# Kernel optimization log

Hardware: AMD Instinct MI355X
Metric: run time of the kernel (lower is better)

Reference implementation:

```python
import jax, jax.numpy as jnp
import numpy as np
import math

P = 2; GS = 64; TPS = 32; T = TPS * TPS; DIM = 256; NH = 8; HD = DIM // NH; NL = 5; FFH = 1024
SCALES = ((0.15, 16), (0.3, 32))
ENC_H = 32; ENC_O = 64
XMIN, XMAX, YMIN, YMAX = -2.0, 4.0, -1.5, 1.5
NFREQ = 10
N_PTS = 20000; N_Q = 100000; G = GS * GS


def rope_tables():
    half = HD // 2
    inv = 1.0 / (10000.0 ** (jnp.arange(0, half, 2, dtype=jnp.float32) / half))  # [HD/4]
    h = jnp.arange(TPS, dtype=jnp.float32)
    w = jnp.arange(TPS, dtype=jnp.float32)
    hg, wg = jnp.meshgrid(h, w, indexing='ij')
    ax = wg.reshape(-1)[:, None] * inv[None, :]  # [T, HD/4]
    ay = hg.reshape(-1)[:, None] * inv[None, :]
    return jnp.cos(ax), jnp.sin(ax), jnp.cos(ay), jnp.sin(ay)


def apply_rope(x, cx, sx, cy, sy):
    B, H, Tn, D = x.shape
    hd = D // 2; pd = hd // 2
    xp = x[..., :hd].reshape(B, H, Tn, pd, 2)
    yp = x[..., hd:].reshape(B, H, Tn, pd, 2)
    cx = cx[None, None]; sx = sx[None, None]; cy = cy[None, None]; sy = sy[None, None]
    rx = jnp.stack([xp[..., 0] * cx - xp[..., 1] * sx, xp[..., 0] * sx + xp[..., 1] * cx], -1).reshape(B, H, Tn, hd)
    ry = jnp.stack([yp[..., 0] * cy - yp[..., 1] * sy, yp[..., 0] * sy + yp[..., 1] * cy], -1).reshape(B, H, Tn, hd)
    return jnp.concatenate([rx, ry], -1)


def rmsnorm(x, w):
    n = jax.lax.rsqrt(jnp.mean(x.astype(jnp.float32) ** 2, -1, keepdims=True) + 1e-6)
    return (x.astype(jnp.float32) * n).astype(x.dtype) * w


def encode_scale(grid, points, radius, k, w1, b1, w2, b2):
    # squared distances [G, N] via gemm (monotone in euclidean dist -> same topk)
    g2 = jnp.sum(grid ** 2, -1, keepdims=True)
    p2 = jnp.sum(points ** 2, -1)
    d2 = g2 + p2[None, :] - 2.0 * (grid @ points.T)
    neg, idx = jax.lax.top_k(-d2, k)  # k nearest
    valid = (-neg) < radius * radius  # [G, k]
    rel = points[idx] - grid[:, None, :]  # [G, k, 2]
    rel = jnp.where(valid[..., None], rel, 0.0)
    h = jax.nn.relu(rel @ w1 + b1)
    f = h @ w2 + b2  # [G, k, ENC_O]
    masked = jnp.where(valid[..., None], f, -jnp.inf)
    pooled = jnp.max(masked, axis=1)
    return jnp.where(jnp.any(valid, axis=1)[:, None], pooled, 0.0)


def fourier_feats(x):
    freqs = (2.0 ** jnp.arange(NFREQ, dtype=jnp.float32)) * math.pi
    scaled = x[..., None] * freqs  # [..., 2, NFREQ]
    enc = jnp.concatenate([jnp.sin(scaled), jnp.cos(scaled)], -1).reshape(*x.shape[:-1], -1)
    return jnp.concatenate([x, enc], -1)  # [..., 2*(1+2*NFREQ)]


def bilinear_sample(feat, xn, yn):
    # feat [C,H,W]; xn,yn in [-1,1]; align_corners=True, border padding
    C, H, W = feat.shape
    px = (xn + 1.0) * 0.5 * (W - 1)
    py = (yn + 1.0) * 0.5 * (H - 1)
    x0 = jnp.clip(jnp.floor(px), 0, W - 1)
    y0 = jnp.clip(jnp.floor(py), 0, H - 1)
    wx = px - x0; wy = py - y0
    x0i = x0.astype(jnp.int32); y0i = y0.astype(jnp.int32)
    x1i = jnp.clip(x0i + 1, 0, W - 1); y1i = jnp.clip(y0i + 1, 0, H - 1)
    f00 = feat[:, y0i, x0i]; f01 = feat[:, y0i, x1i]
    f10 = feat[:, y1i, x0i]; f11 = feat[:, y1i, x1i]
    out = (f00 * (1 - wx) * (1 - wy) + f01 * wx * (1 - wy) + f10 * (1 - wx) * wy + f11 * wx * wy)
    return out.T  # [N, C]


def forward(points, grid, query_pos, query_uinf, query_sdf, query_sdf_grad,
            enc_w1, enc_b1, enc_w2, enc_b2, inproj_w, inproj_b, patch_w, patch_b,
            norm1_w, qkv_w, attnproj_w, norm2_w, gate_w, value_w, ffnout_w,
            unpatch_w, unpatch_b, posmlp_w1, posmlp_b1, posmlp_w2, posmlp_b2,
            pred_w1, pred_b1, pred_w2, pred_b2):
    # --- PointNet multi-scale encoder onto grid ---
    feats = [encode_scale(grid, points, SCALES[i][0], SCALES[i][1],
                          enc_w1[i], enc_b1[i], enc_w2[i], enc_b2[i]) for i in range(len(SCALES))]
    gfeat = jnp.concatenate(feats, -1) @ inproj_w + inproj_b  # [G, DIM]
    img = gfeat.reshape(GS, GS, DIM).transpose(2, 0, 1)[None]  # [1, DIM, GS, GS]
    # --- patchify ---
    x = img.reshape(1, DIM, TPS, P, TPS, P).transpose(0, 2, 4, 1, 3, 5).reshape(1, T, DIM * P * P)
    tok = x @ patch_w + patch_b  # [1, T, DIM]
    cx, sx, cy, sy = rope_tables()
    scale = 1.0 / math.sqrt(HD)
    for l in range(NL):
        h = rmsnorm(tok, norm1_w[l])
        qkv = (h @ qkv_w[l]).reshape(1, T, 3, NH, HD).transpose(2, 0, 3, 1, 4)
        q, k, v = qkv[0], qkv[1], qkv[2]
        q = apply_rope(q, cx, sx, cy, sy)
        k = apply_rope(k, cx, sx, cy, sy)
        att = jax.nn.softmax(jnp.einsum('bhqd,bhkd->bhqk', q, k) * scale, axis=-1)
        o = jnp.einsum('bhqk,bhkd->bhqd', att, v).transpose(0, 2, 1, 3).reshape(1, T, DIM)
        tok = tok + o @ attnproj_w[l]
        h2 = rmsnorm(tok, norm2_w[l])
        tok = tok + (jax.nn.silu(h2 @ gate_w[l]) * (h2 @ value_w[l])) @ ffnout_w[l]
    up = tok @ unpatch_w + unpatch_b  # [1, T, DIM*P*P]
    proc = up.reshape(1, TPS, TPS, DIM, P, P).transpose(0, 3, 1, 4, 2, 5).reshape(1, DIM, GS, GS)
    # --- decoder ---
    xn = jnp.clip(2.0 * (query_pos[:, 0] - XMIN) / (XMAX - XMIN) - 1.0, -1.0, 1.0)
    yn = jnp.clip(2.0 * (query_pos[:, 1] - YMIN) / (YMAX - YMIN) - 1.0, -1.0, 1.0)
    local = bilinear_sample(proc[0], xn, yn)  # [Nq, DIM]
    fp = fourier_feats(jnp.stack([xn, yn], -1))  # [Nq, 42]
    other = jnp.concatenate([query_uinf, query_sdf, query_sdf_grad], -1)  # [Nq, 5]
    pin = jnp.concatenate([fp, other], -1)  # [Nq, 47]
    pe = jax.nn.relu(pin @ posmlp_w1 + posmlp_b1) @ posmlp_w2 + posmlp_b2  # [Nq, 512]
    ctx = jnp.concatenate([local, pe], -1)  # [Nq, 768]
    return jax.nn.relu(ctx @ pred_w1 + pred_b1) @ pred_w2 + pred_b2  # [Nq, 4]


def setup_inputs() -> dict:
    key = jax.random.key(0)
    ks = jax.random.split(key, 32)
    def lin(k, fi, fo, stack=None):
        sh = (fi, fo) if stack is None else (stack, fi, fo)
        return jax.random.normal(k, sh, jnp.float32) / np.sqrt(fi)
    ux = jax.random.uniform(ks[0], (N_PTS, 2), jnp.float32)
    points = jnp.stack([XMIN + ux[:, 0] * (XMAX - XMIN), YMIN + ux[:, 1] * (YMAX - YMIN)], -1)
    gx = jnp.linspace(XMIN, XMAX, GS); gy = jnp.linspace(YMIN, YMAX, GS)
    gyy, gxx = jnp.meshgrid(gy, gx, indexing='ij')
    grid = jnp.stack([gxx.reshape(-1), gyy.reshape(-1)], -1).astype(jnp.float32)  # row-major (H,W)
    uq = jax.random.uniform(ks[1], (N_Q, 2), jnp.float32)
    query_pos = jnp.stack([XMIN + uq[:, 0] * (XMAX - XMIN), YMIN + uq[:, 1] * (YMAX - YMIN)], -1)
    nsc = len(SCALES); pf = DIM * P * P; cdim = 2 * (1 + 2 * NFREQ) + 5
    return {
        'points': points, 'grid': grid, 'query_pos': query_pos,
        'query_uinf': jax.random.normal(ks[2], (N_Q, 2), jnp.float32),
        'query_sdf': jax.random.normal(ks[3], (N_Q, 1), jnp.float32),
        'query_sdf_grad': jax.random.normal(ks[4], (N_Q, 2), jnp.float32),
        'enc_w1': lin(ks[5], 2, ENC_H, nsc), 'enc_b1': jnp.zeros((nsc, ENC_H), jnp.float32),
        'enc_w2': lin(ks[6], ENC_H, ENC_O, nsc), 'enc_b2': jnp.zeros((nsc, ENC_O), jnp.float32),
        'inproj_w': lin(ks[7], ENC_O * nsc, DIM), 'inproj_b': jnp.zeros((DIM,), jnp.float32),
        'patch_w': lin(ks[8], pf, DIM), 'patch_b': jnp.zeros((DIM,), jnp.float32),
        'norm1_w': jnp.ones((NL, DIM), jnp.float32),
        'qkv_w': lin(ks[9], DIM, 3 * DIM, NL),
        'attnproj_w': lin(ks[10], DIM, DIM, NL),
        'norm2_w': jnp.ones((NL, DIM), jnp.float32),
        'gate_w': lin(ks[11], DIM, FFH, NL),
        'value_w': lin(ks[12], DIM, FFH, NL),
        'ffnout_w': lin(ks[13], FFH, DIM, NL),
        'unpatch_w': lin(ks[14], DIM, pf), 'unpatch_b': jnp.zeros((pf,), jnp.float32),
        'posmlp_w1': lin(ks[15], cdim, 256), 'posmlp_b1': jnp.zeros((256,), jnp.float32),
        'posmlp_w2': lin(ks[16], 256, 512), 'posmlp_b2': jnp.zeros((512,), jnp.float32),
        'pred_w1': lin(ks[17], DIM + 512, 256), 'pred_b1': jnp.zeros((256,), jnp.float32),
        'pred_w2': lin(ks[18], 256, 4), 'pred_b2': jnp.zeros((4,), jnp.float32),
    }


def reference(points, grid, query_pos, query_uinf, query_sdf, query_sdf_grad,
              enc_w1, enc_b1, enc_w2, enc_b2, inproj_w, inproj_b, patch_w, patch_b,
              norm1_w, qkv_w, attnproj_w, norm2_w, gate_w, value_w, ffnout_w,
              unpatch_w, unpatch_b, posmlp_w1, posmlp_b1, posmlp_w2, posmlp_b2,
              pred_w1, pred_b1, pred_w2, pred_b2):
    return forward(points, grid, query_pos, query_uinf, query_sdf, query_sdf_grad,
                   enc_w1, enc_b1, enc_w2, enc_b2, inproj_w, inproj_b, patch_w, patch_b,
                   norm1_w, qkv_w, attnproj_w, norm2_w, gate_w, value_w, ffnout_w,
                   unpatch_w, unpatch_b, posmlp_w1, posmlp_b1, posmlp_w2, posmlp_b2,
                   pred_w1, pred_b1, pred_w2, pred_b2)
```

## Files before the change

kernel.cpp:

```cpp
#include <hip/hip_runtime.h>
#include <math.h>

typedef __attribute__((ext_vector_type(8))) short short8;
typedef __attribute__((ext_vector_type(8))) unsigned short ushort8;
typedef __attribute__((ext_vector_type(4))) float f32x4;
typedef __attribute__((ext_vector_type(16))) float f32x16;

#define NPTS  20000
#define NQ    100000
#define TOK   1024
#define DIMD  256
#define NHD   8
#define NLAY  5
#define GRD   4096
#define CAP   512
#define QN    32

#define XMINF (-2.0f)
#define YMINF (-1.5f)
#define CELL  0.15f
#define NCX   40
#define NCY   20
#define NCELL 800

#define MFMA(a,b,c)   __builtin_amdgcn_mfma_f32_16x16x32_bf16(a,b,c,0,0,0)
#define MFMA32(a,b,c) __builtin_amdgcn_mfma_f32_32x32x16_bf16(a,b,c,0,0,0)

__device__ inline void split2(float x, ushort& h, ushort& l) {
  unsigned u = __float_as_uint(x);
  unsigned hr = (u + 0x7FFFu + ((u >> 16) & 1u)) & 0xFFFF0000u;
  h = (ushort)(hr >> 16);
  float r = x - __uint_as_float(hr);
  unsigned u2 = __float_as_uint(r);
  l = (ushort)((u2 + 0x7FFFu + ((u2 >> 16) & 1u)) >> 16);
}

__device__ inline int cell_of(float px, float py) {
  int cx = (int)floorf((px - XMINF) / CELL);
  int cy = (int)floorf((py - YMINF) / CELL);
  cx = min(max(cx, 0), NCX - 1);
  cy = min(max(cy, 0), NCY - 1);
  return cy * NCX + cx;
}

__global__ void k_zero(int* __restrict__ cnt) {
  int i = blockIdx.x * 256 + threadIdx.x;
  if (i < NCELL) cnt[i] = 0;
}

__global__ void k_bincount(const float* __restrict__ pts, int* __restrict__ cnt) {
  int p = blockIdx.x * 256 + threadIdx.x;
  if (p < NPTS) atomicAdd(&cnt[cell_of(pts[p*2], pts[p*2+1])], 1);
}

__global__ void k_prefix(const int* __restrict__ cnt, int* __restrict__ start,
                         int* __restrict__ cursor) {
  __shared__ int s[1024];
  int t = threadIdx.x;
  int v0 = (t < NCELL) ? cnt[t] : 0;
  s[t] = v0;
  __syncthreads();
  for (int off = 1; off < 1024; off <<= 1) {
    int v = (t >= off) ? s[t - off] : 0;
    __syncthreads();
    s[t] += v;
    __syncthreads();
  }
  int ex = s[t] - v0;
  if (t < NCELL) { start[t] = ex; cursor[t] = ex; }
  if (t == 0) start[NCELL] = NPTS;
}

__global__ void k_scatter(const float* __restrict__ pts, int* __restrict__ cursor,
                          float* __restrict__ bpx, float* __restrict__ bpy,
                          int* __restrict__ bpi) {
  int p = blockIdx.x * 256 + threadIdx.x;
  if (p < NPTS) {
    float px = pts[p*2], py = pts[p*2+1];
    int slot = atomicAdd(&cursor[cell_of(px, py)], 1);
    bpx[slot] = px; bpy[slot] = py; bpi[slot] = p;
  }
}

__global__ void k_encode(const float* __restrict__ bpx, const float* __restrict__ bpy,
                         const int* __restrict__ bpi, const int* __restrict__ cellstart,
                         const float* __restrict__ grd,
                         const float* __restrict__ w1, const float* __restrict__ b1,
                         const float* __restrict__ w2, const float* __restrict__ b2,
                         ushort* __restrict__ fH, ushort* __restrict__ fL) {
  __shared__ float s_d2[CAP], s_px[CAP], s_py[CAP];
  __shared__ int   s_idx[CAP];
  __shared__ int   s_cnt;
  __shared__ float s_selx[32], s_sely[32];
  __shared__ float s_part[4][64];

  int gi = blockIdx.x, sc = blockIdx.y;
  int tid = threadIdx.x;
  const float radius = (sc == 0) ? 0.15f : 0.30f;
  const int   K      = (sc == 0) ? 16 : 32;
  float gx = grd[gi*2+0], gy = grd[gi*2+1];
  float g2 = __fadd_rn(__fmul_rn(gx,gx), __fmul_rn(gy,gy));
  float r2 = __fmul_rn(radius, radius);

  if (tid == 0) s_cnt = 0;
  __syncthreads();

  int cx0 = min(max((int)floorf((gx - radius - XMINF) / CELL), 0), NCX - 1);
  int cx1 = min(max((int)floorf((gx + radius - XMINF) / CELL), 0), NCX - 1);
  int cy0 = min(max((int)floorf((gy - radius - YMINF) / CELL), 0), NCY - 1);
  int cy1 = min(max((int)floorf((gy + radius - YMINF) / CELL), 0), NCY - 1);

  for (int cy = cy0; cy <= cy1; ++cy) {
    int b0 = cellstart[cy*NCX + cx0];
    int b1 = cellstart[cy*NCX + cx1 + 1];
    for (int i = b0 + tid; i < b1; i += 256) {
      float px = bpx[i], py = bpy[i];
      float p2  = __fadd_rn(__fmul_rn(px,px), __fmul_rn(py,py));
      float dot = __fadd_rn(__fmul_rn(gx,px), __fmul_rn(gy,py));
      float d2  = __fsub_rn(__fadd_rn(g2,p2), __fmul_rn(2.0f,dot));
      if (d2 < r2) {
        int pos = atomicAdd(&s_cnt, 1);
        if (pos < CAP) { s_d2[pos] = d2; s_px[pos] = px; s_py[pos] = py; s_idx[pos] = bpi[i]; }
      }
    }
  }
  __syncthreads();
  int m = min(s_cnt, CAP);
  int nsel;

  if (m > K) {
    for (int i = tid; i < m; i += 256) {
      float di = s_d2[i];
      int   pi = s_idx[i];
      int rank = 0;
      for (int j = 0; j < m; ++j) {
        float dj = s_d2[j];
        rank += (dj < di || (dj == di && s_idx[j] < pi)) ? 1 : 0;
      }
      if (rank < K) { s_selx[rank] = s_px[i]; s_sely[rank] = s_py[i]; }
    }
    nsel = K;
  } else {
    if (tid < m) { s_selx[tid] = s_px[tid]; s_sely[tid] = s_py[tid]; }
    nsel = m;
  }
  __syncthreads();

  int grp = tid >> 6, d = tid & 63;
  s_part[grp][d] = -INFINITY;
  __syncthreads();
  const float* W1 = w1 + sc*64;
  const float* B1 = b1 + sc*32;
  const float* W2 = w2 + sc*2048;
  const float* B2 = b2 + sc*64;
  for (int base = 0; base < nsel; base += 4) {
    int pi = base + grp;
    if (pi < nsel) {
      float rx = s_selx[pi] - gx;
      float ry = s_sely[pi] - gy;
      float f = B2[d];
      #pragma unroll
      for (int j = 0; j < 32; ++j) {
        float h = rx * W1[j] + ry * W1[32 + j] + B1[j];
        h = fmaxf(h, 0.0f);
        f += h * W2[j*64 + d];
      }
      s_part[grp][d] = fmaxf(s_part[grp][d], f);
    }
  }
  __syncthreads();
  if (tid < 64) {
    float v = fmaxf(fmaxf(s_part[0][tid], s_part[1][tid]),
                    fmaxf(s_part[2][tid], s_part[3][tid]));
    if (nsel == 0) v = 0.0f;
    ushort h, l; split2(v, h, l);
    fH[gi*128 + sc*64 + tid] = h;
    fL[gi*128 + sc*64 + tid] = l;
  }
}

__global__ void k_gemm(const float* __restrict__ A, const float* __restrict__ B,
                       float* __restrict__ C, int M, int N, int K) {
  __shared__ float As[32][33];
  __shared__ float Bs[32][33];
  int bm = blockIdx.y * 32, bn = blockIdx.x * 32;
  int tx = threadIdx.x & 31, ty = threadIdx.x >> 5;
  float acc[4] = {0.f, 0.f, 0.f, 0.f};
  for (int k0 = 0; k0 < K; k0 += 32) {
    for (int i = threadIdx.x; i < 1024; i += 256) {
      int r = i >> 5, c = i & 31;
      As[r][c] = A[(size_t)(bm + r)*K + k0 + c];
      Bs[r][c] = B[(size_t)(k0 + r)*N + bn + c];
    }
    __syncthreads();
    #pragma unroll
    for (int kk = 0; kk < 32; ++kk) {
      float bv = Bs[kk][tx];
      #pragma unroll
      for (int i = 0; i < 4; ++i) acc[i] += As[ty + 8*i][kk] * bv;
    }
    __syncthreads();
  }
  #pragma unroll
  for (int i = 0; i < 4; ++i)
    C[(size_t)(bm + ty + 8*i)*N + bn + tx] = acc[i];
}

__global__ void k_beff(const float* __restrict__ db1, const float* __restrict__ pb2,
                       const float* __restrict__ dw1, float* __restrict__ b2eff) {
  int n = threadIdx.x;
  float a = db1[n];
  for (int j = 0; j < 512; ++j) a += pb2[j] * dw1[(size_t)(256 + j)*256 + n];
  b2eff[n] = a;
}

struct SDesc { const float* src; ushort* dh; ushort* dl; int K, N, Kp, blk0; };
struct STable { int nw; SDesc d[31]; };

__global__ void k_splitT_all(STable tab) {
  __shared__ float tile[32][33];
  int b = blockIdx.x;
  int w = 0;
  for (int i = 1; i < tab.nw; ++i) if (b >= tab.d[i].blk0) w = i;
  SDesc s = tab.d[w];
  int rel = b - s.blk0;
  int ntn = s.N >> 5;
  int tk = rel / ntn, tn = rel - tk*ntn;
  int r = threadIdx.x >> 5, c = threadIdx.x & 31;
  #pragma unroll
  for (int i = 0; i < 4; ++i) {
    int kk = tk*32 + r + i*8;
    tile[r + i*8][c] = (kk < s.K) ? s.src[(size_t)kk*s.N + tn*32 + c] : 0.f;
  }
  __syncthreads();
  #pragma unroll
  for (int i = 0; i < 4; ++i) {
    int nn = tn*32 + r + i*8;
    float v = tile[c][r + i*8];
    ushort hh, ll; split2(v, hh, ll);
    size_t o = (size_t)nn*s.Kp + tk*32 + c;
    s.dh[o] = hh; s.dl[o] = ll;
  }
}

__global__ void k_split(const float* __restrict__ x, ushort* __restrict__ h,
                        ushort* __restrict__ l, int n) {
  int i = blockIdx.x * 256 + threadIdx.x;
  if (i < n) { ushort a, b; split2(x[i], a, b); h[i] = a; l[i] = b; }
}

template<bool BIAS, bool RESID>
__global__ __launch_bounds__(256,2)
void k_mgemm64(const ushort* __restrict__ Ah, const ushort* __restrict__ Al,
               const ushort* __restrict__ Bh, const ushort* __restrict__ Bl,
               const float* __restrict__ bias, const float* __restrict__ resid,
               float* __restrict__ C, int M, int N, int K) {
  __shared__ ushort sAh[64*40], sAl[64*40], sBh[64*40], sBl[64*40];
  int tid = threadIdx.x;
  int wave = tid >> 6, lane = tid & 63, l15 = lane & 15, lhi = lane >> 4;
  int bm = blockIdx.y * 64, bn = blockIdx.x * 64;
  int sr = tid >> 2, sg = (tid & 3) * 8;
  const size_t aoff = (size_t)(bm + sr) * K + sg;
  const size_t boff = (size_t)(bn + sr) * K + sg;
  f32x4 acc[4];
  #pragma unroll
  for (int m = 0; m < 4; ++m) acc[m] = (f32x4){0.f,0.f,0.f,0.f};

  for (int k0 = 0; k0 < K; k0 += 32) {
    __syncthreads();
    *(ushort8*)(sAh + sr*40 + sg) = *(const ushort8*)(Ah + aoff + k0);
    *(ushort8*)(sAl + sr*40 + sg) = *(const ushort8*)(Al + aoff + k0);
    *(ushort8*)(sBh + sr*40 + sg) = *(const ushort8*)(Bh + boff + k0);
    *(ushort8*)(sBl + sr*40 + sg) = *(const ushort8*)(Bl + boff + k0);
    __syncthreads();
    short8 ah[4], al[4];
    #pragma unroll
    for (int m = 0; m < 4; ++m) {
      int r = m*16 + l15;
      ah[m] = *(const short8*)(sAh + r*40 + lhi*8);
      al[m] = *(const short8*)(sAl + r*40 + lhi*8);
    }
    int rb = wave*16 + l15;
    short8 bh = *(const short8*)(sBh + rb*40 + lhi*8);
    short8 bl = *(const short8*)(sBl + rb*40 + lhi*8);
    #pragma unroll
    for (int m = 0; m < 4; ++m) {
      acc[m] = MFMA(ah[m], bh, acc[m]);
      acc[m] = MFMA(al[m], bh, acc[m]);
      acc[m] = MFMA(ah[m], bl, acc[m]);
    }
  }

  int gc = bn + wave*16 + l15;
  float bv = BIAS ? bias[gc] : 0.f;
  #pragma unroll
  for (int m = 0; m < 4; ++m) {
    int gr0 = bm + m*16 + lhi*4;
    #pragma unroll
    for (int r = 0; r < 4; ++r) {
      size_t idx = (size_t)(gr0 + r)*N + gc;
      float v = acc[m][r] + bv;
      if (RESID) v += resid[idx];
      C[idx] = v;
    }
  }
}

__global__ __launch_bounds__(256,2)
void k_ffgv(const ushort* __restrict__ Ah, const ushort* __restrict__ Al,
            const ushort* __restrict__ Bh, const ushort* __restrict__ Bl,
            ushort* __restrict__ fH, ushort* __restrict__ fL) {
  __shared__ ushort sAh[64*40], sAl[64*40];
  __shared__ ushort sGh[64*40], sGl[64*40];
  __shared__ ushort sVh[64*40], sVl[64*40];
  int tid = threadIdx.x;
  int wave = tid >> 6, lane = tid & 63, l15 = lane & 15, lhi = lane >> 4;
  int bm = blockIdx.y * 64, bn = blockIdx.x * 64;
  int sr = tid >> 2, sg = (tid & 3) * 8;
  const size_t aoff = (size_t)(bm + sr) * 256 + sg;
  const size_t goff = (size_t)(bn + sr) * 256 + sg;
  const size_t voff = (size_t)(1024 + bn + sr) * 256 + sg;
  f32x4 accg[4], accv[4];
  #pragma unroll
  for (int m = 0; m < 4; ++m) { accg[m] = (f32x4){0.f,0.f,0.f,0.f}; accv[m] = accg[m]; }

  for (int k0 = 0; k0 < 256; k0 += 32) {
    __syncthreads();
    *(ushort8*)(sAh + sr*40 + sg) = *(const ushort8*)(Ah + aoff + k0);
    *(ushort8*)(sAl + sr*40 + sg) = *(const ushort8*)(Al + aoff + k0);
    *(ushort8*)(sGh + sr*40 + sg) = *(const ushort8*)(Bh + goff + k0);
    *(ushort8*)(sGl + sr*40 + sg) = *(const ushort8*)(Bl + goff + k0);
    *(ushort8*)(sVh + sr*40 + sg) = *(const ushort8*)(Bh + voff + k0);
    *(ushort8*)(sVl + sr*40 + sg) = *(const ushort8*)(Bl + voff + k0);
    __syncthreads();
    short8 ah[4], al[4];
    #pragma unroll
    for (int m = 0; m < 4; ++m) {
      int r = m*16 + l15;
      ah[m] = *(const short8*)(sAh + r*40 + lhi*8);
      al[m] = *(const short8*)(sAl + r*40 + lhi*8);
    }
    int rb = wave*16 + l15;
    short8 gh = *(const short8*)(sGh + rb*40 + lhi*8);
    short8 gl = *(const short8*)(sGl + rb*40 + lhi*8);
    short8 vh = *(const short8*)(sVh + rb*40 + lhi*8);
    short8 vl = *(const short8*)(sVl + rb*40 + lhi*8);
    #pragma unroll
    for (int m = 0; m < 4; ++m) {
      accg[m] = MFMA(ah[m], gh, accg[m]);
      accg[m] = MFMA(al[m], gh, accg[m]);
      accg[m] = MFMA(ah[m], gl, accg[m]);
      accv[m] = MFMA(ah[m], vh, accv[m]);
      accv[m] = MFMA(al[m], vh, accv[m]);
      accv[m] = MFMA(ah[m], vl, accv[m]);
    }
  }

  int gc = bn + wave*16 + l15;
  #pragma unroll
  for (int m = 0; m < 4; ++m) {
    int gr0 = bm + m*16 + lhi*4;
    #pragma unroll
    for (int r = 0; r < 4; ++r) {
      float g = accg[m][r], v = accv[m][r];
      float s = g / (1.0f + expf(-g));
      float rr = s * v;
      ushort hh, ll; split2(rr, hh, ll);
      size_t idx = (size_t)(gr0 + r)*1024 + gc;
      fH[idx] = hh; fL[idx] = ll;
    }
  }
}

__global__ void k_patchgather(const float* __restrict__ gfeat,
                              ushort* __restrict__ xH, ushort* __restrict__ xL) {
  int i = blockIdx.x * 256 + threadIdx.x;
  int t = i >> 10, f = i & 1023;
  int ty = t >> 5, tx = t & 31;
  int c = f >> 2, py = (f >> 1) & 1, px = f & 1;
  float v = gfeat[(size_t)((ty*2 + py)*64 + (tx*2 + px))*DIMD + c];
  ushort h, l; split2(v, h, l);
  xH[i] = h; xL[i] = l;
}

__global__ void k_unpatch(const float* __restrict__ up,
                          ushort* __restrict__ pH, ushort* __restrict__ pL) {
  int i = blockIdx.x * 256 + threadIdx.x;
  int c = i & 255; int yx = i >> 8; int x = yx & 63; int y = yx >> 6;
  float v = up[(size_t)((y>>1)*32 + (x>>1))*1024 + (c<<2) + ((y&1)<<1) + (x&1)];
  ushort h, l; split2(v, h, l);
  pH[i] = h; pL[i] = l;
}

__global__ void k_rmsnorm_split(const float* __restrict__ x, const float* __restrict__ w,
                                ushort* __restrict__ yH, ushort* __restrict__ yL) {
  __shared__ float red[256];
  int row = blockIdx.x, t = threadIdx.x;
  float v = x[(size_t)row*DIMD + t];
  red[t] = v * v;
  __syncthreads();
  for (int off = 128; off; off >>= 1) {
    if (t < off) red[t] += red[t + off];
    __syncthreads();
  }
  float n = 1.0f / sqrtf(red[0] / 256.0f + 1e-6f);
  float y = v * n * w[t];
  ushort h, l; split2(y, h, l);
  yH[(size_t)row*DIMD + t] = h;
  yL[(size_t)row*DIMD + t] = l;
}

__global__ void k_qkvprep(const float* __restrict__ qkv,
                          ushort* __restrict__ QsH, ushort* __restrict__ QsL,
                          ushort* __restrict__ KsH, ushort* __restrict__ KsL,
                          ushort* __restrict__ VtH, ushort* __restrict__ VtL) {
  int t = blockIdx.x;
  int c = threadIdx.x;
  int h = c >> 5, d = c & 31;
  const float* row = qkv + (size_t)t*768;

  float v = row[512 + c];
  ushort vh, vl; split2(v, vh, vl);
  size_t vo = (size_t)h*32768 + (size_t)d*1024 + t;
  VtH[vo] = vh; VtL[vo] = vl;

  int half = d >> 4, dd = d & 15, pd = dd >> 1, odd = dd & 1;
  float pos = (float)(half ? (t >> 5) : (t & 31));
  float inv = powf(10.0f, -0.5f * (float)pd);
  float ang = pos * inv;
  float cs = cosf(ang), sn = sinf(ang);
  int pbase = h*32 + half*16 + 2*pd;

  float a = row[pbase], b = row[pbase + 1];
  float qv = odd ? (a*sn + b*cs) : (a*cs - b*sn);
  qv *= 0.17677669529663687f;
  size_t qo = (size_t)h*32768 + (size_t)t*32 + d;
  ushort qh_, ql_; split2(qv, qh_, ql_);
  QsH[qo] = qh_; QsL[qo] = ql_;

  float a2 = row[256 + pbase], b2 = row[256 + pbase + 1];
  float kv = odd ? (a2*sn + b2*cs) : (a2*cs - b2*sn);
  ushort kh_, kl_; split2(kv, kh_, kl_);
  KsH[qo] = kh_; KsL[qo] = kl_;
}

__global__ __launch_bounds__(512,1)
void k_fattn(const ushort* __restrict__ QsH, const ushort* __restrict__ QsL,
             const ushort* __restrict__ KsH, const ushort* __restrict__ KsL,
             const ushort* __restrict__ VtH, const ushort* __restrict__ VtL,
             ushort* __restrict__ oH, ushort* __restrict__ oL) {
  __shared__ float sM[8][64], sL[8][64];
  __shared__ float sO[8][64][16];
  int h  = blockIdx.x >> 5;
  int qt = blockIdx.x & 31;
  int tid = threadIdx.x;
  int wv = tid >> 6, lane = tid & 63;
  int l31 = lane & 31, lhi = (lane >> 5) & 1;

  const size_t qoff = ((size_t)h*1024 + qt*32 + l31)*32 + lhi*8;
  short8 qh = *(const short8*)(QsH + qoff);
  short8 ql = *(const short8*)(QsL + qoff);

  f32x16 oacc;
  #pragma unroll
  for (int r = 0; r < 16; ++r) oacc[r] = 0.f;
  float mrun = -INFINITY, lrun = 0.f;

  for (int kt = wv*4; kt < wv*4 + 4; ++kt) {
    const size_t koff = ((size_t)h*1024 + kt*32 + l31)*32 + lhi*8;
    short8 kh = *(const short8*)(KsH + koff);
    short8 kl = *(const short8*)(KsL + koff);
    const size_t voff = ((size_t)h*32 + l31)*1024 + kt*32 + lhi*8;
    short8 vh0 = *(const short8*)(VtH + voff);
    short8 vl0 = *(const short8*)(VtL + voff);
    short8 vh1 = *(const short8*)(VtH + voff + 16);
    short8 vl1 = *(const short8*)(VtL + voff + 16);

    f32x16 s;
    #pragma unroll
    for (int r = 0; r < 16; ++r) s[r] = 0.f;
    s = MFMA32(kh, qh, s);
    s = MFMA32(kl, qh, s);
    s = MFMA32(kh, ql, s);

    float mloc = s[0];
    #pragma unroll
    for (int r = 1; r < 16; ++r) mloc = fmaxf(mloc, s[r]);
    mloc = fmaxf(mloc, __shfl_xor(mloc, 32));
    float mnew = fmaxf(mrun, mloc);
    float fsc = __expf(mrun - mnew);
    float p[16]; float ssum = 0.f;
    #pragma unroll
    for (int r = 0; r < 16; ++r) { p[r] = __expf(s[r] - mnew); ssum += p[r]; }
    ssum += __shfl_xor(ssum, 32);
    lrun = lrun * fsc + ssum;
    mrun = mnew;
    #pragma unroll
    for (int r = 0; r < 16; ++r) oacc[r] *= fsc;

    unsigned wh[8], wl[8];
    #pragma unroll
    for (int i = 0; i < 8; ++i) {
      ushort h0,l0,h1,l1;
      split2(p[2*i], h0, l0);
      split2(p[2*i+1], h1, l1);
      wh[i] = (unsigned)h0 | ((unsigned)h1 << 16);
      wl[i] = (unsigned)l0 | ((unsigned)l1 << 16);
    }
    unsigned pwh[8], pwl[8];
    #pragma unroll
    for (int i = 0; i < 8; ++i) {
      pwh[i] = (unsigned)__shfl_xor((int)wh[i], 32);
      pwl[i] = (unsigned)__shfl_xor((int)wl[i], 32);
    }
    union U { unsigned u[4]; short8 s; };
    U bh0, bl0, bh1, bl1;
    bh0.u[0] = lhi ? pwh[2] : wh[0];  bh0.u[1] = lhi ? pwh[3] : wh[1];
    bh0.u[2] = lhi ? wh[2]  : pwh[0]; bh0.u[3] = lhi ? wh[3]  : pwh[1];
    bl0.u[0] = lhi ? pwl[2] : wl[0];  bl0.u[1] = lhi ? pwl[3] : wl[1];
    bl0.u[2] = lhi ? wl[2]  : pwl[0]; bl0.u[3] = lhi ? wl[3]  : pwl[1];
    bh1.u[0] = lhi ? pwh[6] : wh[4];  bh1.u[1] = lhi ? pwh[7] : wh[5];
    bh1.u[2] = lhi ? wh[6]  : pwh[4]; bh1.u[3] = lhi ? wh[7]  : pwh[5];
    bl1.u[0] = lhi ? pwl[6] : wl[4];  bl1.u[1] = lhi ? pwl[7] : wl[5];
    bl1.u[2] = lhi ? wl[6]  : pwl[4]; bl1.u[3] = lhi ? wl[7]  : pwl[5];

    oacc = MFMA32(vh0, bh0.s, oacc);
    oacc = MFMA32(vl0, bh0.s, oacc);
    oacc = MFMA32(vh0, bl0.s, oacc);
    oacc = MFMA32(vh1, bh1.s, oacc);
    oacc = MFMA32(vl1, bh1.s, oacc);
    oacc = MFMA32(vh1, bl1.s, oacc);
  }

  sM[wv][lane] = mrun;
  sL[wv][lane] = lrun;
  #pragma unroll
  for (int r = 0; r < 16; ++r) sO[wv][lane][r] = oacc[r];
  __syncthreads();

  if (wv == 0) {
    float M = sM[0][lane];
    #pragma unroll
    for (int w = 1; w < 8; ++w) M = fmaxf(M, sM[w][lane]);
    float L = 0.f;
    float O[16];
    #pragma unroll
    for (int r = 0; r < 16; ++r) O[r] = 0.f;
    #pragma unroll
    for (int w = 0; w < 8; ++w) {
      float f = __expf(sM[w][lane] - M);
      L += sL[w][lane] * f;
      #pragma unroll
      for (int r = 0; r < 16; ++r) O[r] += sO[w][lane][r] * f;
    }
    float inv = 1.0f / L;
    int t = qt*32 + l31;
    #pragma unroll
    for (int r = 0; r < 16; ++r) {
      int d = (r & 3) + 8*(r >> 2) + 4*lhi;
      float v = O[r] * inv;
      ushort hh, ll; split2(v, hh, ll);
      oH[(size_t)t*DIMD + h*32 + d] = hh;
      oL[(size_t)t*DIMD + h*32 + d] = ll;
    }
  }
}

__global__ __launch_bounds__(256,3)
void k_qhead(const float* __restrict__ qpos, const float* __restrict__ quinf,
             const float* __restrict__ qsdf, const float* __restrict__ qgrad,
             const float* __restrict__ projCL,
             const ushort* __restrict__ pw1tH, const ushort* __restrict__ pw1tL,
             const float* __restrict__ pb1,
             const ushort* __restrict__ wcH, const ushort* __restrict__ wcL,
             const float* __restrict__ b2eff,
             const float* __restrict__ dw2, const float* __restrict__ db2,
             float* __restrict__ out) {
  __shared__ ushort sPinH[QN*72], sPinL[QN*72];
  __shared__ char   sBig[QN*264*2*2];
  __shared__ float  sXY[QN][2];
  __shared__ float  sDW2[1024];
  ushort* sH1H = (ushort*)sBig;
  ushort* sH1L = sH1H + QN*264;
  float*  sH2  = (float*)sBig;

  int tid = threadIdx.x;
  int wave = tid >> 6, lane = tid & 63, l15 = lane & 15, lhi = lane >> 4;
  int q0 = blockIdx.x * QN;

  for (int i = tid; i < 1024; i += 256) sDW2[i] = dw2[i];

  if (tid < QN) {
    int qg = min(q0 + tid, NQ - 1);
    float x = qpos[(size_t)qg*2 + 0], y = qpos[(size_t)qg*2 + 1];
    float xn = fminf(fmaxf(2.0f*(x + 2.0f)/6.0f - 1.0f, -1.0f), 1.0f);
    float yn = fminf(fmaxf(2.0f*(y + 1.5f)/3.0f - 1.0f, -1.0f), 1.0f);
    sXY[tid][0] = xn; sXY[tid][1] = yn;
  }
  __syncthreads();

  {
    int q = tid >> 3;
    int j0 = (tid & 7) * 8;
    int qg = min(q0 + q, NQ - 1);
    float xn = sXY[q][0], yn = sXY[q][1];
    for (int jj = 0; jj < 8; ++jj) {
      int j = j0 + jj;
      float v = 0.f;
      if (j == 0) v = xn;
      else if (j == 1) v = yn;
      else if (j < 42) {
        int z = j - 2;
        int coord = z / 20;
        int w = z % 20;
        int isCos = w / 10;
        int fi = w % 10;
        float f = ldexpf(3.14159265358979323846f, fi);
        float a = (coord ? yn : xn) * f;
        v = isCos ? cosf(a) : sinf(a);
      }
      else if (j < 44) v = quinf[(size_t)qg*2 + (j-42)];
      else if (j == 44) v = qsdf[qg];
      else if (j < 47) v = qgrad[(size_t)qg*2 + (j-45)];
      ushort h, l; split2(v, h, l);
      sPinH[q*72 + j] = h; sPinL[q*72 + j] = l;
    }
  }
  __syncthreads();

  f32x4 acc[2][4];
  #pragma unroll
  for (int m = 0; m < 2; ++m)
    #pragma unroll
    for (int n = 0; n < 4; ++n) acc[m][n] = (f32x4){0.f,0.f,0.f,0.f};

  for (int ks = 0; ks < 2; ++ks) {
    short8 bh[4], bl[4];
    #pragma unroll
    for (int n = 0; n < 4; ++n) {
      int r = wave*64 + n*16 + l15;
      bh[n] = *(const short8*)(pw1tH + r*64 + ks*32 + lhi*8);
      bl[n] = *(const short8*)(pw1tL + r*64 + ks*32 + lhi*8);
    }
    short8 ah[2], al[2];
    #pragma unroll
    for (int m = 0; m < 2; ++m) {
      int r = m*16 + l15;
      ah[m] = *(const short8*)(sPinH + r*72 + ks*32 + lhi*8);
      al[m] = *(const short8*)(sPinL + r*72 + ks*32 + lhi*8);
    }
    #pragma unroll
    for (int m = 0; m < 2; ++m)
      #pragma unroll
      for (int n = 0; n < 4; ++n) {
        acc[m][n] = MFMA(ah[m], bh[n], acc[m][n]);
        acc[m][n] = MFMA(al[m], bh[n], acc[m][n]);
        acc[m][n] = MFMA(ah[m], bl[n], acc[m][n]);
      }
  }
  #pragma unroll
  for (int m = 0; m < 2; ++m) {
    #pragma unroll
    for (int n = 0; n < 4; ++n) {
      int col = wave*64 + n*16 + l15;
      float bv = pb1[col];
      #pragma unroll
      for (int r = 0; r < 4; ++r) {
        int row = m*16 + lhi*4 + r;
        float v = fmaxf(acc[m][n][r] + bv, 0.f);
        ushort h, l; split2(v, h, l);
        sH1H[row*264 + col] = h;
        sH1L[row*264 + col] = l;
      }
      acc[m][n] = (f32x4){0.f,0.f,0.f,0.f};
    }
  }
  __syncthreads();

  for (int ks = 0; ks < 8; ++ks) {
    short8 bh[4], bl[4];
    #pragma unroll
    for (int n = 0; n < 4; ++n) {
      int r = wave*64 + n*16 + l15;
      bh[n] = *(const short8*)(wcH + (size_t)r*256 + ks*32 + lhi*8);
      bl[n] = *(const short8*)(wcL + (size_t)r*256 + ks*32 + lhi*8);
    }
    short8 ah[2], al[2];
    #pragma unroll
    for (int m = 0; m < 2; ++m) {
      int r = m*16 + l15;
      ah[m] = *(const short8*)(sH1H + r*264 + ks*32 + lhi*8);
      al[m] = *(const short8*)(sH1L + r*264 + ks*32 + lhi*8);
    }
    #pragma unroll
    for (int m = 0; m < 2; ++m)
      #pragma unroll
      for (int n = 0; n < 4; ++n) {
        acc[m][n] = MFMA(ah[m], bh[n], acc[m][n]);
        acc[m][n] = MFMA(al[m], bh[n], acc[m][n]);
        acc[m][n] = MFMA(ah[m], bl[n], acc[m][n]);
      }
  }
  __syncthreads();

  #pragma unroll
  for (int m = 0; m < 2; ++m) {
    #pragma unroll
    for (int r = 0; r < 4; ++r) {
      int q = m*16 + lhi*4 + r;
      float xn = sXY[q][0], yn = sXY[q][1];
      float px = (xn + 1.0f) * 0.5f * 63.0f;
      float py = (yn + 1.0f) * 0.5f * 63.0f;
      float x0 = fminf(fmaxf(floorf(px), 0.f), 63.f);
      float y0 = fminf(fmaxf(floorf(py), 0.f), 63.f);
      float wx = px - x0, wy = py - y0;
      int x0i = (int)x0, y0i = (int)y0;
      int x1i = min(x0i + 1, 63), y1i = min(y0i + 1, 63);
      const float* p00 = projCL + (size_t)(y0i*64 + x0i)*256;
      const float* p01 = projCL + (size_t)(y0i*64 + x1i)*256;
      const float* p10 = projCL + (size_t)(y1i*64 + x0i)*256;
      const float* p11 = projCL + (size_t)(y1i*64 + x1i)*256;
      float w00 = (1.f-wx)*(1.f-wy), w01 = wx*(1.f-wy), w10 = (1.f-wx)*wy, w11 = wx*wy;
      #pragma unroll
      for (int n = 0; n < 4; ++n) {
        int col = wave*64 + n*16 + l15;
        float bil = w00*p00[col] + w01*p01[col] + w10*p10[col] + w11*p11[col];
        float v = acc[m][n][r] + b2eff[col] + bil;
        sH2[q*264 + col] = fmaxf(v, 0.f);
      }
    }
  }
  __syncthreads();

  if (tid < QN*4) {
    int q = tid >> 2, d = tid & 3;
    float a = db2[d];
    for (int j = 0; j < 256; ++j) a += sH2[q*264 + j] * sDW2[j*4 + d];
    out[(size_t)(q0 + q)*4 + d] = a;
  }
}

extern "C" void kernel_launch(void* const* d_in, const int* in_sizes, int n_in,
                              void* d_out, int out_size, void* d_ws, size_t ws_size,
                              hipStream_t stream) {
  (void)in_sizes; (void)n_in; (void)out_size; (void)ws_size;
  const float* points     = (const float*)d_in[0];
  const float* grd        = (const float*)d_in[1];
  const float* qpos       = (const float*)d_in[2];
  const float* quinf      = (const float*)d_in[3];
  const float* qsdf       = (const float*)d_in[4];
  const float* qgrad      = (const float*)d_in[5];
  const float* enc_w1     = (const float*)d_in[6];
  const float* enc_b1     = (const float*)d_in[7];
  const float* enc_w2     = (const float*)d_in[8];
  const float* enc_b2     = (const float*)d_in[9];
  const float* inproj_w   = (const float*)d_in[10];
  const float* inproj_b   = (const float*)d_in[11];
  const float* patch_w    = (const float*)d_in[12];
  const float* patch_b    = (const float*)d_in[13];
  const float* norm1_w    = (const float*)d_in[14];
  const float* qkv_w      = (const float*)d_in[15];
  const float* attnproj_w = (const float*)d_in[16];
  const float* norm2_w    = (const float*)d_in[17];
  const float* gate_w     = (const float*)d_in[18];
  const float* value_w    = (const float*)d_in[19];
  const float* ffnout_w   = (const float*)d_in[20];
  const float* unpatch_w  = (const float*)d_in[21];
  const float* unpatch_b  = (const float*)d_in[22];
  const float* pw1        = (const float*)d_in[23];
  const float* pb1        = (const float*)d_in[24];
  const float* pw2        = (const float*)d_in[25];
  const float* pb2        = (const float*)d_in[26];
  const float* dw1        = (const float*)d_in[27];
  const float* db1        = (const float*)d_in[28];
  const float* dw2        = (const float*)d_in[29];
  const float* db2        = (const float*)d_in[30];
  float* out = (float*)d_out;

  char* base = (char*)d_ws;
  size_t off = 0;
  auto alloc = [&](size_t bytes) -> void* {
    void* p = base + off; off += (bytes + 255) & ~(size_t)255; return p;
  };

  ushort* inprojTH = (ushort*)alloc(32768*2);   ushort* inprojTL = (ushort*)alloc(32768*2);
  ushort* patchTH  = (ushort*)alloc(262144*2);  ushort* patchTL  = (ushort*)alloc(262144*2);
  ushort* upTH     = (ushort*)alloc(262144*2);  ushort* upTL     = (ushort*)alloc(262144*2);
  ushort* pw1TH    = (ushort*)alloc(16384*2);   ushort* pw1TL    = (ushort*)alloc(16384*2);
  ushort* wcTH     = (ushort*)alloc(65536*2);   ushort* wcTL     = (ushort*)alloc(65536*2);
  ushort* dw1aTH   = (ushort*)alloc(65536*2);   ushort* dw1aTL   = (ushort*)alloc(65536*2);
  float*  Wcomb    = (float*)alloc(65536*4);
  float*  b2eff    = (float*)alloc(256*4);

  int*   cellcnt   = (int*)alloc(NCELL*4);
  int*   cellstart = (int*)alloc((NCELL+1)*4);
  int*   cursor    = (int*)alloc(NCELL*4);
  float* bpx       = (float*)alloc(NPTS*4);
  float* bpy       = (float*)alloc(NPTS*4);
  int*   bpi       = (int*)alloc(NPTS*4);

  ushort* lwH = (ushort*)alloc((size_t)NLAY*1048576*2);
  ushort* lwL = (ushort*)alloc((size_t)NLAY*1048576*2);
  const size_t qkvO = 0, apO = 196608, gateO = 262144, foO = 786432;

  ushort* xpH = (ushort*)alloc(1048576*2);
  ushort* xpL = (ushort*)alloc(1048576*2);
  float*  tok = (float*)alloc(262144*4);
  ushort* hH  = (ushort*)alloc(262144*2);
  ushort* hL  = (ushort*)alloc(262144*2);
  float*  qkvb = (float*)alloc(786432*4);
  ushort* oH  = (ushort*)alloc(262144*2);
  ushort* oL  = (ushort*)alloc(262144*2);
  float*  unionBuf = (float*)alloc(2097152*4);
  float*  gfeat  = unionBuf;
  float*  projCL = unionBuf + 1048576;

  ushort* QsH = (ushort*)unionBuf;
  ushort* QsL = QsH + 262144;
  ushort* KsH = QsH + 2*262144;
  ushort* KsL = QsH + 3*262144;
  ushort* VtH = QsH + 4*262144;
  ushort* VtL = QsH + 5*262144;

  ushort* featcH = xpH;  ushort* featcL = xpL;
  ushort* ffH    = xpH;  ushort* ffL    = xpL;
  ushort* prH    = xpH;  ushort* prL    = xpL;
  ushort* tkH    = hH;   ushort* tkL    = hL;

  k_gemm<<<dim3(8,8), 256, 0, stream>>>(pw2, dw1 + 256*256, Wcomb, 256, 256, 512);
  k_beff<<<1, 256, 0, stream>>>(db1, pb2, dw1, b2eff);

  auto addw = [](STable& t, int& cb, const float* src, ushort* dh, ushort* dl,
                 int K, int N, int Kp) {
    SDesc& s = t.d[t.nw]; s.src = src; s.dh = dh; s.dl = dl;
    s.K = K; s.N = N; s.Kp = Kp; s.blk0 = cb;
    cb += (Kp >> 5) * (N >> 5); t.nw++;
  };

  {
    STable gt; gt.nw = 0; int cb = 0;
    addw(gt, cb, inproj_w, inprojTH, inprojTL, 128, 256, 128);
    addw(gt, cb, patch_w,  patchTH,  patchTL,  1024, 256, 1024);
    addw(gt, cb, unpatch_w, upTH, upTL, 256, 1024, 256);
    addw(gt, cb, pw1,   pw1TH,  pw1TL,  47, 256, 64);
    addw(gt, cb, Wcomb, wcTH,   wcTL,   256, 256, 256);
    addw(gt, cb, dw1,   dw1aTH, dw1aTL, 256, 256, 256);
    for (int l = 0; l < NLAY; ++l) {
      size_t lb = (size_t)l*1048576;
      addw(gt, cb, qkv_w      + (size_t)l*196608, lwH + lb + qkvO,  lwL + lb + qkvO,  256, 768, 256);
      addw(gt, cb, attnproj_w + (size_t)l*65536,  lwH + lb + apO,   lwL + lb + apO,   256, 256, 256);
      addw(gt, cb, gate_w     + (size_t)l*262144, lwH + lb + gateO,          lwL + lb + gateO,          256, 1024, 256);
      addw(gt, cb, value_w    + (size_t)l*262144, lwH + lb + gateO + 262144, lwL + lb + gateO + 262144, 256, 1024, 256);
      addw(gt, cb, ffnout_w   + (size_t)l*262144, lwH + lb + foO,   lwL + lb + foO,   1024, 256, 1024);
    }
    k_splitT_all<<<cb, 256, 0, stream>>>(gt);
  }

  k_zero<<<4, 256, 0, stream>>>(cellcnt);
  k_bincount<<<(NPTS+255)/256, 256, 0, stream>>>(points, cellcnt);
  k_prefix<<<1, 1024, 0, stream>>>(cellcnt, cellstart, cursor);
  k_scatter<<<(NPTS+255)/256, 256, 0, stream>>>(points, cursor, bpx, bpy, bpi);

  k_encode<<<dim3(GRD, 2), 256, 0, stream>>>(bpx, bpy, bpi, cellstart, grd,
                                             enc_w1, enc_b1, enc_w2, enc_b2, featcH, featcL);
  k_mgemm64<true,false><<<dim3(4,64), 256, 0, stream>>>(featcH, featcL, inprojTH, inprojTL, inproj_b, nullptr, gfeat, GRD, 256, 128);
  k_patchgather<<<4096, 256, 0, stream>>>(gfeat, xpH, xpL);
  k_mgemm64<true,false><<<dim3(4,16), 256, 0, stream>>>(xpH, xpL, patchTH, patchTL, patch_b, nullptr, tok, TOK, 256, 1024);

  for (int l = 0; l < NLAY; ++l) {
    size_t lb = (size_t)l*1048576;
    k_rmsnorm_split<<<TOK, 256, 0, stream>>>(tok, norm1_w + (size_t)l*DIMD, hH, hL);
    k_mgemm64<false,false><<<dim3(12,16), 256, 0, stream>>>(hH, hL, lwH + lb + qkvO, lwL + lb + qkvO, nullptr, nullptr, qkvb, TOK, 768, 256);
    k_qkvprep<<<1024, 256, 0, stream>>>(qkvb, QsH, QsL, KsH, KsL, VtH, VtL);
    k_fattn<<<256, 512, 0, stream>>>(QsH, QsL, KsH, KsL, VtH, VtL, oH, oL);
    k_mgemm64<false,true><<<dim3(4,16), 256, 0, stream>>>(oH, oL, lwH + lb + apO, lwL + lb + apO, nullptr, tok, tok, TOK, 256, 256);
    k_rmsnorm_split<<<TOK, 256, 0, stream>>>(tok, norm2_w + (size_t)l*DIMD, hH, hL);
    k_ffgv<<<dim3(16,16), 256, 0, stream>>>(hH, hL, lwH + lb + gateO, lwL + lb + gateO, ffH, ffL);
    k_mgemm64<false,true><<<dim3(4,16), 256, 0, stream>>>(ffH, ffL, lwH + lb + foO, lwL + lb + foO, nullptr, tok, tok, TOK, 256, 1024);
  }

  k_split<<<1024, 256, 0, stream>>>(tok, tkH, tkL, 262144);
  k_mgemm64<true,false><<<dim3(16,16), 256, 0, stream>>>(tkH, tkL, upTH, upTL, unpatch_b, nullptr, gfeat, TOK, 1024, 256);
  k_unpatch<<<4096, 256, 0, stream>>>(gfeat, prH, prL);
  k_mgemm64<false,false><<<dim3(4,64), 256, 0, stream>>>(prH, prL, dw1aTH, dw1aTL, nullptr, nullptr, projCL, GRD, 256, 256);

  k_qhead<<<NQ/QN, 256, 0, stream>>>(qpos, quinf, qsdf, qgrad, projCL,
      pw1TH, pw1TL, pb1, wcTH, wcTL, b2eff, dw2, db2, out);
}
```

Baseline: 771.4 us.

## Fuse layout transforms and RoPE into GEMM epilogues, widen query head kernel

Moves patch-gather, unpatch, the final split, and QKV RoPE/transpose preparation into the epilogues of the neighbouring GEMMs. This removes several standalone kernels and their fp32 intermediate round trips through global memory. The query head now launches 512 threads and folds the final 256-to-4 projection into per-wave shuffle reductions instead of a shared-memory staging pass. The trade-off is scattered, uncoalesced stores in the fused epilogues, and the RoPE path now uses the fast __sinf/__cosf intrinsics.

```diff
diff --git a/kernel.cpp b/kernel.cpp
--- a/kernel.cpp
+++ b/kernel.cpp
@@ -3,6 +3,7 @@
 
 typedef __attribute__((ext_vector_type(8))) short short8;
 typedef __attribute__((ext_vector_type(8))) unsigned short ushort8;
+typedef __attribute__((ext_vector_type(4))) unsigned short ushort4v;
 typedef __attribute__((ext_vector_type(4))) float f32x4;
 typedef __attribute__((ext_vector_type(16))) float f32x16;
 
@@ -243,18 +244,13 @@
   }
 }
 
-__global__ void k_split(const float* __restrict__ x, ushort* __restrict__ h,
-                        ushort* __restrict__ l, int n) {
-  int i = blockIdx.x * 256 + threadIdx.x;
-  if (i < n) { ushort a, b; split2(x[i], a, b); h[i] = a; l[i] = b; }
-}
-
-template<bool BIAS, bool RESID>
+template<bool BIAS, bool RESID, bool WSPLIT>
 __global__ __launch_bounds__(256,2)
 void k_mgemm64(const ushort* __restrict__ Ah, const ushort* __restrict__ Al,
                const ushort* __restrict__ Bh, const ushort* __restrict__ Bl,
                const float* __restrict__ bias, const float* __restrict__ resid,
-               float* __restrict__ C, int M, int N, int K) {
+               float* __restrict__ C, int M, int N, int K,
+               ushort* __restrict__ wsH, ushort* __restrict__ wsL) {
   __shared__ ushort sAh[64*40], sAl[64*40], sBh[64*40], sBl[64*40];
   int tid = threadIdx.x;
   int wave = tid >> 6, lane = tid & 63, l15 = lane & 15, lhi = lane >> 4;
@@ -302,6 +298,363 @@
       float v = acc[m][r] + bv;
       if (RESID) v += resid[idx];
       C[idx] = v;
+      if (WSPLIT) {
+        ushort hh, ll; split2(v, hh, ll);
+        wsH[idx] = hh; wsL[idx] = ll;
+      }
+    }
+  }
+}
+
+__global__ __launch_bounds__(256,2)
+void k_inproj(const ushort* __restrict__ Ah, const ushort* __restrict__ Al,
+              const ushort* __restrict__ Bh, const ushort* __restrict__ Bl,
+              const float* __restrict__ bias,
+              ushort* __restrict__ xH, ushort* __restrict__ xL) {
+  __shared__ ushort sAh[64*40], sAl[64*40], sBh[64*40], sBl[64*40];
+  int tid = threadIdx.x;
+  int wave = tid >> 6, lane = tid & 63, l15 = lane & 15, lhi = lane >> 4;
+  int bm = blockIdx.y * 64, bn = blockIdx.x * 64;
+  int sr = tid >> 2, sg = (tid & 3) * 8;
+  const int K = 128;
+  const size_t aoff = (size_t)(bm + sr) * K + sg;
+  const size_t boff = (size_t)(bn + sr) * K + sg;
+  f32x4 acc[4];
+  #pragma unroll
+  for (int m = 0; m < 4; ++m) acc[m] = (f32x4){0.f,0.f,0.f,0.f};
+
+  for (int k0 = 0; k0 < K; k0 += 32) {
+    __syncthreads();
+    *(ushort8*)(sAh + sr*40 + sg) = *(const ushort8*)(Ah + aoff + k0);
+    *(ushort8*)(sAl + sr*40 + sg) = *(const ushort8*)(Al + aoff + k0);
+    *(ushort8*)(sBh + sr*40 + sg) = *(const ushort8*)(Bh + boff + k0);
+    *(ushort8*)(sBl + sr*40 + sg) = *(const ushort8*)(Bl + boff + k0);
+    __syncthreads();
+    short8 ah[4], al[4];
+    #pragma unroll
+    for (int m = 0; m < 4; ++m) {
+      int r = m*16 + l15;
+      ah[m] = *(const short8*)(sAh + r*40 + lhi*8);
+      al[m] = *(const short8*)(sAl + r*40 + lhi*8);
+    }
+    int rb = wave*16 + l15;
+    short8 bh = *(const short8*)(sBh + rb*40 + lhi*8);
+    short8 bl = *(const short8*)(sBl + rb*40 + lhi*8);
+    #pragma unroll
+    for (int m = 0; m < 4; ++m) {
+      acc[m] = MFMA(ah[m], bh, acc[m]);
+      acc[m] = MFMA(al[m], bh, acc[m]);
+      acc[m] = MFMA(ah[m], bl, acc[m]);
+    }
+  }
+
+  int gc = bn + wave*16 + l15;
+  float bv = bias[gc];
+  #pragma unroll
+  for (int m = 0; m < 4; ++m) {
+    int gr0 = bm + m*16 + lhi*4;
+    #pragma unroll
+    for (int r = 0; r < 4; ++r) {
+      int g = gr0 + r;
+      int y = g >> 6, x = g & 63;
+      int t = (y >> 1)*32 + (x >> 1);
+      int f = gc*4 + (y & 1)*2 + (x & 1);
+      float v = acc[m][r] + bv;
+      ushort hh, ll; split2(v, hh, ll);
+      size_t o = (size_t)t*1024 + f;
+      xH[o] = hh; xL[o] = ll;
+    }
+  }
+}
+
+__global__ __launch_bounds__(256,2)
+void k_upgemm(const ushort* __restrict__ Ah, const ushort* __restrict__ Al,
+              const ushort* __restrict__ Bh, const ushort* __restrict__ Bl,
+              const float* __restrict__ bias,
+              ushort* __restrict__ pH, ushort* __restrict__ pL) {
+  __shared__ ushort sAh[64*40], sAl[64*40], sBh[64*40], sBl[64*40];
+  int tid = threadIdx.x;
+  int wave = tid >> 6, lane = tid & 63, l15 = lane & 15, lhi = lane >> 4;
+  int bm = blockIdx.y * 64, bn = blockIdx.x * 64;
+  int sr = tid >> 2, sg = (tid & 3) * 8;
+  const int K = 256;
+  const size_t aoff = (size_t)(bm + sr) * K + sg;
+  const size_t boff = (size_t)(bn + sr) * K + sg;
+  f32x4 acc[4];
+  #pragma unroll
+  for (int m = 0; m < 4; ++m) acc[m] = (f32x4){0.f,0.f,0.f,0.f};
+
+  for (int k0 = 0; k0 < K; k0 += 32) {
+    __syncthreads();
+    *(ushort8*)(sAh + sr*40 + sg) = *(const ushort8*)(Ah + aoff + k0);
+    *(ushort8*)(sAl + sr*40 + sg) = *(const ushort8*)(Al + aoff + k0);
+    *(ushort8*)(sBh + sr*40 + sg) = *(const ushort8*)(Bh + boff + k0);
+    *(ushort8*)(sBl + sr*40 + sg) = *(const ushort8*)(Bl + boff + k0);
+    __syncthreads();
+    short8 ah[4], al[4];
+    #pragma unroll
+    for (int m = 0; m < 4; ++m) {
+      int r = m*16 + l15;
+      ah[m] = *(const short8*)(sAh + r*40 + lhi*8);
+      al[m] = *(const short8*)(sAl + r*40 + lhi*8);
+    }
+    int rb = wave*16 + l15;
+    short8 bh = *(const short8*)(sBh + rb*40 + lhi*8);
+    short8 bl = *(const short8*)(sBl + rb*40 + lhi*8);
+    #pragma unroll
+    for (int m = 0; m < 4; ++m) {
+      acc[m] = MFMA(ah[m], bh, acc[m]);
+      acc[m] = MFMA(al[m], bh, acc[m]);
+      acc[m] = MFMA(ah[m], bl, acc[m]);
+    }
+  }
+
+  int u = bn + wave*16 + l15;
+  float bv = bias[u];
+  int c  = u >> 2;
+  int py = (u >> 1) & 1, px = u & 1;
+  #pragma unroll
+  for (int m = 0; m < 4; ++m) {
+    int gr0 = bm + m*16 + lhi*4;
+    #pragma unroll
+    for (int r = 0; r < 4; ++r) {
+      int t = gr0 + r;
+      int y = (t >> 5)*2 + py, x = (t & 31)*2 + px;
+      float v = acc[m][r] + bv;
+      ushort hh, ll; split2(v, hh, ll);
+      size_t o = (size_t)(y*64 + x)*256 + c;
+      pH[o] = hh; pL[o] = ll;
+    }
+  }
+}
+
+__global__ __launch_bounds__(256,2)
+void k_qkvrope(const ushort* __restrict__ Ah, const ushort* __restrict__ Al,
+               const ushort* __restrict__ Bh, const ushort* __restrict__ Bl,
+               ushort* __restrict__ QsH, ushort* __restrict__ QsL,
+               ushort* __restrict__ KsH, ushort* __restrict__ KsL,
+               ushort* __restrict__ VtH, ushort* __restrict__ VtL) {
+  __shared__ ushort sAh[64*40], sAl[64*40], sBh[64*40], sBl[64*40];
+  int tid = threadIdx.x;
+  int wave = tid >> 6, lane = tid & 63, l15 = lane & 15, lhi = lane >> 4;
+  int bm = blockIdx.y * 64, bn = blockIdx.x * 64;
+  int sr = tid >> 2, sg = (tid & 3) * 8;
+  const int K = 256, N = 768;
+  const size_t aoff = (size_t)(bm + sr) * K + sg;
+  const size_t boff = (size_t)(bn + sr) * K + sg;
+  f32x4 acc[4];
+  #pragma unroll
+  for (int m = 0; m < 4; ++m) acc[m] = (f32x4){0.f,0.f,0.f,0.f};
+  (void)N;
+
+  for (int k0 = 0; k0 < K; k0 += 32) {
+    __syncthreads();
+    *(ushort8*)(sAh + sr*40 + sg) = *(const ushort8*)(Ah + aoff + k0);
+    *(ushort8*)(sAl + sr*40 + sg) = *(const ushort8*)(Al + aoff + k0);
+    *(ushort8*)(sBh + sr*40 + sg) = *(const ushort8*)(Bh + boff + k0);
+    *(ushort8*)(sBl + sr*40 + sg) = *(const ushort8*)(Bl + boff + k0);
+    __syncthreads();
+    short8 ah[4], al[4];
+    #pragma unroll
+    for (int m = 0; m < 4; ++m) {
+      int r = m*16 + l15;
+      ah[m] = *(const short8*)(sAh + r*40 + lhi*8);
+      al[m] = *(const short8*)(sAl + r*40 + lhi*8);
+    }
+    int rb = wave*16 + l15;
+    short8 bh = *(const short8*)(sBh + rb*40 + lhi*8);
+    short8 bl = *(const short8*)(sBl + rb*40 + lhi*8);
+    #pragma unroll
+    for (int m = 0; m < 4; ++m) {
+      acc[m] = MFMA(ah[m], bh, acc[m]);
+      acc[m] = MFMA(al[m], bh, acc[m]);
+      acc[m] = MFMA(ah[m], bl, acc[m]);
+    }
+  }
+
+  int gc = bn + wave*16 + l15;
+  if (gc < 512) {
+    int qk = gc >> 8;
+    int c  = gc & 255;
+    int h  = c >> 5, d = c & 31;
+    int half = d >> 4, dd = d & 15, pd = dd >> 1, odd = dd & 1;
+    float inv = powf(10.0f, -0.5f * (float)pd);
+    float scl = qk ? 1.0f : 0.17677669529663687f;
+    ushort* dH = qk ? KsH : QsH;
+    ushort* dL = qk ? KsL : QsL;
+    #pragma unroll
+    for (int m = 0; m < 4; ++m) {
+      int gr0 = bm + m*16 + lhi*4;
+      #pragma unroll
+      for (int r = 0; r < 4; ++r) {
+        int t = gr0 + r;
+        float v = acc[m][r];
+        float pv = __shfl_xor(v, 1);
+        float pos = (float)(half ? (t >> 5) : (t & 31));
+        float ang = pos * inv;
+        float cs = __cosf(ang), sn = __sinf(ang);
+        float res = odd ? (pv*sn + v*cs) : (v*cs - pv*sn);
+        res *= scl;
+        ushort hh, ll; split2(res, hh, ll);
+        size_t o = (size_t)h*32768 + (size_t)t*32 + d;
+        dH[o] = hh; dL[o] = ll;
+      }
+    }
+  } else {
+    int c = gc - 512;
+    int h = c >> 5, d = c & 31;
+    #pragma unroll
+    for (int m = 0; m < 4; ++m) {
+      int t0 = bm + m*16 + lhi*4;
+      ushort4v vh, vl;
+      #pragma unroll
+      for (int r = 0; r < 4; ++r) {
+        ushort hh, ll; split2(acc[m][r], hh, ll);
+        vh[r] = hh; vl[r] = ll;
+      }
+      size_t o = (size_t)h*32768 + (size_t)d*1024 + t0;
+      *(ushort4v*)(VtH + o) = vh;
+      *(ushort4v*)(VtL + o) = vl;
+    }
+  }
+}
+
+__global__ void k_rmsnorm_split(const float* __restrict__ x, const float* __restrict__ w,
+                                ushort* __restrict__ yH, ushort* __restrict__ yL) {
+  __shared__ float red[256];
+  int row = blockIdx.x, t = threadIdx.x;
+  float v = x[(size_t)row*DIMD + t];
+  red[t] = v * v;
+  __syncthreads();
+  for (int off = 128; off; off >>= 1) {
+    if (t < off) red[t] += red[t + off];
+    __syncthreads();
+  }
+  float n = 1.0f / sqrtf(red[0] / 256.0f + 1e-6f);
+  float y = v * n * w[t];
+  ushort h, l; split2(y, h, l);
+  yH[(size_t)row*DIMD + t] = h;
+  yL[(size_t)row*DIMD + t] = l;
+}
+
+__global__ __launch_bounds__(512,1)
+void k_fattn(const ushort* __restrict__ QsH, const ushort* __restrict__ QsL,
+             const ushort* __restrict__ KsH, const ushort* __restrict__ KsL,
+             const ushort* __restrict__ VtH, const ushort* __restrict__ VtL,
+             ushort* __restrict__ oH, ushort* __restrict__ oL) {
+  __shared__ float sM[8][64], sL[8][64];
+  __shared__ float sO[8][64][16];
+  int h  = blockIdx.x >> 5;
+  int qt = blockIdx.x & 31;
+  int tid = threadIdx.x;
+  int wv = tid >> 6, lane = tid & 63;
+  int l31 = lane & 31, lhi = (lane >> 5) & 1;
+
+  const size_t qoff = ((size_t)h*1024 + qt*32 + l31)*32 + lhi*8;
+  short8 qh = *(const short8*)(QsH + qoff);
+  short8 ql = *(const short8*)(QsL + qoff);
+
+  f32x16 oacc;
+  #pragma unroll
+  for (int r = 0; r < 16; ++r) oacc[r] = 0.f;
+  float mrun = -INFINITY, lrun = 0.f;
+
+  for (int kt = wv*4; kt < wv*4 + 4; ++kt) {
+    const size_t koff = ((size_t)h*1024 + kt*32 + l31)*32 + lhi*8;
+    short8 kh = *(const short8*)(KsH + koff);
+    short8 kl = *(const short8*)(KsL + koff);
+    const size_t voff = ((size_t)h*32 + l31)*1024 + kt*32 + lhi*8;
+    short8 vh0 = *(const short8*)(VtH + voff);
+    short8 vl0 = *(const short8*)(VtL + voff);
+    short8 vh1 = *(const short8*)(VtH + voff + 16);
+    short8 vl1 = *(const short8*)(VtL + voff + 16);
+
+    f32x16 s;
+    #pragma unroll
+    for (int r = 0; r < 16; ++r) s[r] = 0.f;
+    s = MFMA32(kh, qh, s);
+    s = MFMA32(kl, qh, s);
+    s = MFMA32(kh, ql, s);
+
+    float mloc = s[0];
+    #pragma unroll
+    for (int r = 1; r < 16; ++r) mloc = fmaxf(mloc, s[r]);
+    mloc = fmaxf(mloc, __shfl_xor(mloc, 32));
+    float mnew = fmaxf(mrun, mloc);
+    float fsc = __expf(mrun - mnew);
+    float p[16]; float ssum = 0.f;
+    #pragma unroll
+    for (int r = 0; r < 16; ++r) { p[r] = __expf(s[r] - mnew); ssum += p[r]; }
+    ssum += __shfl_xor(ssum, 32);
+    lrun = lrun * fsc + ssum;
+    mrun = mnew;
+    #pragma unroll
+    for (int r = 0; r < 16; ++r) oacc[r] *= fsc;
+
+    unsigned wh[8], wl[8];
+    #pragma unroll
+    for (int i = 0; i < 8; ++i) {
+      ushort h0,l0,h1,l1;
+      split2(p[2*i], h0, l0);
+      split2(p[2*i+1], h1, l1);
+      wh[i] = (unsigned)h0 | ((unsigned)h1 << 16);
+      wl[i] = (unsigned)l0 | ((unsigned)l1 << 16);
+    }
+    unsigned pwh[8], pwl[8];
+    #pragma unroll
+    for (int i = 0; i < 8; ++i) {
+      pwh[i] = (unsigned)__shfl_xor((int)wh[i], 32);
+      pwl[i] = (unsigned)__shfl_xor((int)wl[i], 32);
+    }
+    union U { unsigned u[4]; short8 s; };
+    U bh0, bl0, bh1, bl1;
+    bh0.u[0] = lhi ? pwh[2] : wh[0];  bh0.u[1] = lhi ? pwh[3] : wh[1];
+    bh0.u[2] = lhi ? wh[2]  : pwh[0]; bh0.u[3] = lhi ? wh[3]  : pwh[1];
+    bl0.u[0] = lhi ? pwl[2] : wl[0];  bl0.u[1] = lhi ? pwl[3] : wl[1];
+    bl0.u[2] = lhi ? wl[2]  : pwl[0]; bl0.u[3] = lhi ? wl[3]  : pwl[1];
+    bh1.u[0] = lhi ? pwh[6] : wh[4];  bh1.u[1] = lhi ? pwh[7] : wh[5];
+    bh1.u[2] = lhi ? wh[6]  : pwh[4]; bh1.u[3] = lhi ? wh[7]  : pwh[5];
+    bl1.u[0] = lhi ? pwl[6] : wl[4];  bl1.u[1] = lhi ? pwl[7] : wl[5];
+    bl1.u[2] = lhi ? wl[6]  : pwl[4]; bl1.u[3] = lhi ? wl[7]  : pwl[5];
+
+    oacc = MFMA32(vh0, bh0.s, oacc);
+    oacc = MFMA32(vl0, bh0.s, oacc);
+    oacc = MFMA32(vh0, bl0.s, oacc);
+    oacc = MFMA32(vh1, bh1.s, oacc);
+    oacc = MFMA32(vl1, bh1.s, oacc);
+    oacc = MFMA32(vh1, bl1.s, oacc);
+  }
+
+  sM[wv][lane] = mrun;
+  sL[wv][lane] = lrun;
+  #pragma unroll
+  for (int r = 0; r < 16; ++r) sO[wv][lane][r] = oacc[r];
+  __syncthreads();
+
+  if (wv == 0) {
+    float M = sM[0][lane];
+    #pragma unroll
+    for (int w = 1; w < 8; ++w) M = fmaxf(M, sM[w][lane]);
+    float L = 0.f;
+    float O[16];
+    #pragma unroll
+    for (int r = 0; r < 16; ++r) O[r] = 0.f;
+    #pragma unroll
+    for (int w = 0; w < 8; ++w) {
+      float f = __expf(sM[w][lane] - M);
+      L += sL[w][lane] * f;
+      #pragma unroll
+      for (int r = 0; r < 16; ++r) O[r] += sO[w][lane][r] * f;
+    }
+    float inv = 1.0f / L;
+    int t = qt*32 + l31;
+    #pragma unroll
+    for (int r = 0; r < 16; ++r) {
+      int d = (r & 3) + 8*(r >> 2) + 4*lhi;
+      float v = O[r] * inv;
+      ushort hh, ll; split2(v, hh, ll);
+      oH[(size_t)t*DIMD + h*32 + d] = hh;
+      oL[(size_t)t*DIMD + h*32 + d] = ll;
     }
   }
 }
@@ -372,201 +725,7 @@
   }
 }
 
-__global__ void k_patchgather(const float* __restrict__ gfeat,
-                              ushort* __restrict__ xH, ushort* __restrict__ xL) {
-  int i = blockIdx.x * 256 + threadIdx.x;
-  int t = i >> 10, f = i & 1023;
-  int ty = t >> 5, tx = t & 31;
-  int c = f >> 2, py = (f >> 1) & 1, px = f & 1;
-  float v = gfeat[(size_t)((ty*2 + py)*64 + (tx*2 + px))*DIMD + c];
-  ushort h, l; split2(v, h, l);
-  xH[i] = h; xL[i] = l;
-}
-
-__global__ void k_unpatch(const float* __restrict__ up,
-                          ushort* __restrict__ pH, ushort* __restrict__ pL) {
-  int i = blockIdx.x * 256 + threadIdx.x;
-  int c = i & 255; int yx = i >> 8; int x = yx & 63; int y = yx >> 6;
-  float v = up[(size_t)((y>>1)*32 + (x>>1))*1024 + (c<<2) + ((y&1)<<1) + (x&1)];
-  ushort h, l; split2(v, h, l);
-  pH[i] = h; pL[i] = l;
-}
-
-__global__ void k_rmsnorm_split(const float* __restrict__ x, const float* __restrict__ w,
-                                ushort* __restrict__ yH, ushort* __restrict__ yL) {
-  __shared__ float red[256];
-  int row = blockIdx.x, t = threadIdx.x;
-  float v = x[(size_t)row*DIMD + t];
-  red[t] = v * v;
-  __syncthreads();
-  for (int off = 128; off; off >>= 1) {
-    if (t < off) red[t] += red[t + off];
-    __syncthreads();
-  }
-  float n = 1.0f / sqrtf(red[0] / 256.0f + 1e-6f);
-  float y = v * n * w[t];
-  ushort h, l; split2(y, h, l);
-  yH[(size_t)row*DIMD + t] = h;
-  yL[(size_t)row*DIMD + t] = l;
-}
-
-__global__ void k_qkvprep(const float* __restrict__ qkv,
-                          ushort* __restrict__ QsH, ushort* __restrict__ QsL,
-                          ushort* __restrict__ KsH, ushort* __restrict__ KsL,
-                          ushort* __restrict__ VtH, ushort* __restrict__ VtL) {
-  int t = blockIdx.x;
-  int c = threadIdx.x;
-  int h = c >> 5, d = c & 31;
-  const float* row = qkv + (size_t)t*768;
-
-  float v = row[512 + c];
-  ushort vh, vl; split2(v, vh, vl);
-  size_t vo = (size_t)h*32768 + (size_t)d*1024 + t;
-  VtH[vo] = vh; VtL[vo] = vl;
-
-  int half = d >> 4, dd = d & 15, pd = dd >> 1, odd = dd & 1;
-  float pos = (float)(half ? (t >> 5) : (t & 31));
-  float inv = powf(10.0f, -0.5f * (float)pd);
-  float ang = pos * inv;
-  float cs = cosf(ang), sn = sinf(ang);
-  int pbase = h*32 + half*16 + 2*pd;
-
-  float a = row[pbase], b = row[pbase + 1];
-  float qv = odd ? (a*sn + b*cs) : (a*cs - b*sn);
-  qv *= 0.17677669529663687f;
-  size_t qo = (size_t)h*32768 + (size_t)t*32 + d;
-  ushort qh_, ql_; split2(qv, qh_, ql_);
-  QsH[qo] = qh_; QsL[qo] = ql_;
-
-  float a2 = row[256 + pbase], b2 = row[256 + pbase + 1];
-  float kv = odd ? (a2*sn + b2*cs) : (a2*cs - b2*sn);
-  ushort kh_, kl_; split2(kv, kh_, kl_);
-  KsH[qo] = kh_; KsL[qo] = kl_;
-}
-
-__global__ __launch_bounds__(512,1)
-void k_fattn(const ushort* __restrict__ QsH, const ushort* __restrict__ QsL,
-             const ushort* __restrict__ KsH, const ushort* __restrict__ KsL,
-             const ushort* __restrict__ VtH, const ushort* __restrict__ VtL,
-             ushort* __restrict__ oH, ushort* __restrict__ oL) {
-  __shared__ float sM[8][64], sL[8][64];
-  __shared__ float sO[8][64][16];
-  int h  = blockIdx.x >> 5;
-  int qt = blockIdx.x & 31;
-  int tid = threadIdx.x;
-  int wv = tid >> 6, lane = tid & 63;
-  int l31 = lane & 31, lhi = (lane >> 5) & 1;
-
-  const size_t qoff = ((size_t)h*1024 + qt*32 + l31)*32 + lhi*8;
-  short8 qh = *(const short8*)(QsH + qoff);
-  short8 ql = *(const short8*)(QsL + qoff);
-
-  f32x16 oacc;
-  #pragma unroll
-  for (int r = 0; r < 16; ++r) oacc[r] = 0.f;
-  float mrun = -INFINITY, lrun = 0.f;
-
-  for (int kt = wv*4; kt < wv*4 + 4; ++kt) {
-    const size_t koff = ((size_t)h*1024 + kt*32 + l31)*32 + lhi*8;
-    short8 kh = *(const short8*)(KsH + koff);
-    short8 kl = *(const short8*)(KsL + koff);
-    const size_t voff = ((size_t)h*32 + l31)*1024 + kt*32 + lhi*8;
-    short8 vh0 = *(const short8*)(VtH + voff);
-    short8 vl0 = *(const short8*)(VtL + voff);
-    short8 vh1 = *(const short8*)(VtH + voff + 16);
-    short8 vl1 = *(const short8*)(VtL + voff + 16);
-
-    f32x16 s;
-    #pragma unroll
-    for (int r = 0; r < 16; ++r) s[r] = 0.f;
-    s = MFMA32(kh, qh, s);
-    s = MFMA32(kl, qh, s);
-    s = MFMA32(kh, ql, s);
-
-    float mloc = s[0];
-    #pragma unroll
-    for (int r = 1; r < 16; ++r) mloc = fmaxf(mloc, s[r]);
-    mloc = fmaxf(mloc, __shfl_xor(mloc, 32));
-    float mnew = fmaxf(mrun, mloc);
-    float fsc = __expf(mrun - mnew);
-    float p[16]; float ssum = 0.f;
-    #pragma unroll
-    for (int r = 0; r < 16; ++r) { p[r] = __expf(s[r] - mnew); ssum += p[r]; }
-    ssum += __shfl_xor(ssum, 32);
-    lrun = lrun * fsc + ssum;
-    mrun = mnew;
-    #pragma unroll
-    for (int r = 0; r < 16; ++r) oacc[r] *= fsc;
-
-    unsigned wh[8], wl[8];
-    #pragma unroll
-    for (int i = 0; i < 8; ++i) {
-      ushort h0,l0,h1,l1;
-      split2(p[2*i], h0, l0);
-      split2(p[2*i+1], h1, l1);
-      wh[i] = (unsigned)h0 | ((unsigned)h1 << 16);
-      wl[i] = (unsigned)l0 | ((unsigned)l1 << 16);
-    }
-    unsigned pwh[8], pwl[8];
-    #pragma unroll
-    for (int i = 0; i < 8; ++i) {
-      pwh[i] = (unsigned)__shfl_xor((int)wh[i], 32);
-      pwl[i] = (unsigned)__shfl_xor((int)wl[i], 32);
-    }
-    union U { unsigned u[4]; short8 s; };
-    U bh0, bl0, bh1, bl1;
-    bh0.u[0] = lhi ? pwh[2] : wh[0];  bh0.u[1] = lhi ? pwh[3] : wh[1];
-    bh0.u[2] = lhi ? wh[2]  : pwh[0]; bh0.u[3] = lhi ? wh[3]  : pwh[1];
-    bl0.u[0] = lhi ? pwl[2] : wl[0];  bl0.u[1] = lhi ? pwl[3] : wl[1];
-    bl0.u[2] = lhi ? wl[2]  : pwl[0]; bl0.u[3] = lhi ? wl[3]  : pwl[1];
-    bh1.u[0] = lhi ? pwh[6] : wh[4];  bh1.u[1] = lhi ? pwh[7] : wh[5];
-    bh1.u[2] = lhi ? wh[6]  : pwh[4]; bh1.u[3] = lhi ? wh[7]  : pwh[5];
-    bl1.u[0] = lhi ? pwl[6] : wl[4];  bl1.u[1] = lhi ? pwl[7] : wl[5];
-    bl1.u[2] = lhi ? wl[6]  : pwl[4]; bl1.u[3] = lhi ? wl[7]  : pwl[5];
-
-    oacc = MFMA32(vh0, bh0.s, oacc);
-    oacc = MFMA32(vl0, bh0.s, oacc);
-    oacc = MFMA32(vh0, bl0.s, oacc);
-    oacc = MFMA32(vh1, bh1.s, oacc);
-    oacc = MFMA32(vl1, bh1.s, oacc);
-    oacc = MFMA32(vh1, bl1.s, oacc);
-  }
-
-  sM[wv][lane] = mrun;
-  sL[wv][lane] = lrun;
-  #pragma unroll
-  for (int r = 0; r < 16; ++r) sO[wv][lane][r] = oacc[r];
-  __syncthreads();
-
-  if (wv == 0) {
-    float M = sM[0][lane];
-    #pragma unroll
-    for (int w = 1; w < 8; ++w) M = fmaxf(M, sM[w][lane]);
-    float L = 0.f;
-    float O[16];
-    #pragma unroll
-    for (int r = 0; r < 16; ++r) O[r] = 0.f;
-    #pragma unroll
-    for (int w = 0; w < 8; ++w) {
-      float f = __expf(sM[w][lane] - M);
-      L += sL[w][lane] * f;
-      #pragma unroll
-      for (int r = 0; r < 16; ++r) O[r] += sO[w][lane][r] * f;
-    }
-    float inv = 1.0f / L;
-    int t = qt*32 + l31;
-    #pragma unroll
-    for (int r = 0; r < 16; ++r) {
-      int d = (r & 3) + 8*(r >> 2) + 4*lhi;
-      float v = O[r] * inv;
-      ushort hh, ll; split2(v, hh, ll);
-      oH[(size_t)t*DIMD + h*32 + d] = hh;
-      oL[(size_t)t*DIMD + h*32 + d] = ll;
-    }
-  }
-}
-
-__global__ __launch_bounds__(256,3)
+__global__ __launch_bounds__(512,4)
 void k_qhead(const float* __restrict__ qpos, const float* __restrict__ quinf,
              const float* __restrict__ qsdf, const float* __restrict__ qgrad,
              const float* __restrict__ projCL,
@@ -577,21 +736,16 @@
              const float* __restrict__ dw2, const float* __restrict__ db2,
              float* __restrict__ out) {
   __shared__ ushort sPinH[QN*72], sPinL[QN*72];
-  __shared__ char   sBig[QN*264*2*2];
+  __shared__ ushort sH1H[QN*264], sH1L[QN*264];
   __shared__ float  sXY[QN][2];
-  __shared__ float  sDW2[1024];
-  ushort* sH1H = (ushort*)sBig;
-  ushort* sH1L = sH1H + QN*264;
-  float*  sH2  = (float*)sBig;
+  __shared__ float  sRed[8][128];
 
   int tid = threadIdx.x;
-  int wave = tid >> 6, lane = tid & 63, l15 = lane & 15, lhi = lane >> 4;
+  int w = tid >> 6, lane = tid & 63, l15 = lane & 15, lhi = lane >> 4;
   int q0 = blockIdx.x * QN;
 
-  for (int i = tid; i < 1024; i += 256) sDW2[i] = dw2[i];
-
   if (tid < QN) {
-    int qg = min(q0 + tid, NQ - 1);
+    int qg = q0 + tid;
     float x = qpos[(size_t)qg*2 + 0], y = qpos[(size_t)qg*2 + 1];
     float xn = fminf(fmaxf(2.0f*(x + 2.0f)/6.0f - 1.0f, -1.0f), 1.0f);
     float yn = fminf(fmaxf(2.0f*(y + 1.5f)/3.0f - 1.0f, -1.0f), 1.0f);
@@ -600,11 +754,12 @@
   __syncthreads();
 
   {
-    int q = tid >> 3;
-    int j0 = (tid & 7) * 8;
-    int qg = min(q0 + q, NQ - 1);
+    int q = tid >> 4;
+    int j0 = (tid & 15) * 4;
+    int qg = q0 + q;
     float xn = sXY[q][0], yn = sXY[q][1];
-    for (int jj = 0; jj < 8; ++jj) {
+    #pragma unroll
+    for (int jj = 0; jj < 4; ++jj) {
       int j = j0 + jj;
       float v = 0.f;
       if (j == 0) v = xn;
@@ -612,12 +767,12 @@
       else if (j < 42) {
         int z = j - 2;
         int coord = z / 20;
-        int w = z % 20;
-        int isCos = w / 10;
-        int fi = w % 10;
+        int ww = z % 20;
+        int isCos = ww / 10;
+        int fi = ww % 10;
         float f = ldexpf(3.14159265358979323846f, fi);
         float a = (coord ? yn : xn) * f;
-        v = isCos ? cosf(a) : sinf(a);
+        v = isCos ? __cosf(a) : __sinf(a);
       }
       else if (j < 44) v = quinf[(size_t)qg*2 + (j-42)];
       else if (j == 44) v = qsdf[qg];
@@ -628,17 +783,18 @@
   }
   __syncthreads();
 
-  f32x4 acc[2][4];
+  f32x4 acc[2][2];
   #pragma unroll
   for (int m = 0; m < 2; ++m)
     #pragma unroll
-    for (int n = 0; n < 4; ++n) acc[m][n] = (f32x4){0.f,0.f,0.f,0.f};
-
+    for (int n = 0; n < 2; ++n) acc[m][n] = (f32x4){0.f,0.f,0.f,0.f};
+
+  #pragma unroll
   for (int ks = 0; ks < 2; ++ks) {
-    short8 bh[4], bl[4];
-    #pragma unroll
-    for (int n = 0; n < 4; ++n) {
-      int r = wave*64 + n*16 + l15;
+    short8 bh[2], bl[2];
+    #pragma unroll
+    for (int n = 0; n < 2; ++n) {
+      int r = w*32 + n*16 + l15;
       bh[n] = *(const short8*)(pw1tH + r*64 + ks*32 + lhi*8);
       bl[n] = *(const short8*)(pw1tL + r*64 + ks*32 + lhi*8);
     }
@@ -652,7 +808,7 @@
     #pragma unroll
     for (int m = 0; m < 2; ++m)
       #pragma unroll
-      for (int n = 0; n < 4; ++n) {
+      for (int n = 0; n < 2; ++n) {
         acc[m][n] = MFMA(ah[m], bh[n], acc[m][n]);
         acc[m][n] = MFMA(al[m], bh[n], acc[m][n]);
         acc[m][n] = MFMA(ah[m], bl[n], acc[m][n]);
@@ -661,8 +817,8 @@
   #pragma unroll
   for (int m = 0; m < 2; ++m) {
     #pragma unroll
-    for (int n = 0; n < 4; ++n) {
-      int col = wave*64 + n*16 + l15;
+    for (int n = 0; n < 2; ++n) {
+      int col = w*32 + n*16 + l15;
       float bv = pb1[col];
       #pragma unroll
       for (int r = 0; r < 4; ++r) {
@@ -677,11 +833,12 @@
   }
   __syncthreads();
 
+  #pragma unroll
   for (int ks = 0; ks < 8; ++ks) {
-    short8 bh[4], bl[4];
-    #pragma unroll
-    for (int n = 0; n < 4; ++n) {
-      int r = wave*64 + n*16 + l15;
+    short8 bh[2], bl[2];
+    #pragma unroll
+    for (int n = 0; n < 2; ++n) {
+      int r = w*32 + n*16 + l15;
       bh[n] = *(const short8*)(wcH + (size_t)r*256 + ks*32 + lhi*8);
       bl[n] = *(const short8*)(wcL + (size_t)r*256 + ks*32 + lhi*8);
     }
@@ -695,13 +852,20 @@
     #pragma unroll
     for (int m = 0; m < 2; ++m)
       #pragma unroll
-      for (int n = 0; n < 4; ++n) {
+      for (int n = 0; n < 2; ++n) {
         acc[m][n] = MFMA(ah[m], bh[n], acc[m][n]);
         acc[m][n] = MFMA(al[m], bh[n], acc[m][n]);
         acc[m][n] = MFMA(ah[m], bl[n], acc[m][n]);
       }
   }
-  __syncthreads();
+
+  float part[2][4][4];
+  #pragma unroll
+  for (int m = 0; m < 2; ++m)
+    #pragma unroll
+    for (int r = 0; r < 4; ++r)
+      #pragma unroll
+      for (int d = 0; d < 4; ++d) part[m][r][d] = 0.f;
 
   #pragma unroll
   for (int m = 0; m < 2; ++m) {
@@ -722,20 +886,47 @@
       const float* p11 = projCL + (size_t)(y1i*64 + x1i)*256;
       float w00 = (1.f-wx)*(1.f-wy), w01 = wx*(1.f-wy), w10 = (1.f-wx)*wy, w11 = wx*wy;
       #pragma unroll
-      for (int n = 0; n < 4; ++n) {
-        int col = wave*64 + n*16 + l15;
+      for (int n = 0; n < 2; ++n) {
+        int col = w*32 + n*16 + l15;
         float bil = w00*p00[col] + w01*p01[col] + w10*p10[col] + w11*p11[col];
-        float v = acc[m][n][r] + b2eff[col] + bil;
-        sH2[q*264 + col] = fmaxf(v, 0.f);
+        float v = fmaxf(acc[m][n][r] + b2eff[col] + bil, 0.f);
+        f32x4 wv = *(const f32x4*)(dw2 + col*4);
+        part[m][r][0] += v * wv[0];
+        part[m][r][1] += v * wv[1];
+        part[m][r][2] += v * wv[2];
+        part[m][r][3] += v * wv[3];
       }
     }
   }
-  __syncthreads();
-
-  if (tid < QN*4) {
+
+  #pragma unroll
+  for (int bit = 1; bit <= 8; bit <<= 1) {
+    #pragma unroll
+    for (int m = 0; m < 2; ++m)
+      #pragma unroll
+      for (int r = 0; r < 4; ++r)
+        #pragma unroll
+        for (int d = 0; d < 4; ++d)
+          part[m][r][d] += __shfl_xor(part[m][r][d], bit);
+  }
+  if (l15 == 0) {
+    #pragma unroll
+    for (int m = 0; m < 2; ++m)
+      #pragma unroll
+      for (int r = 0; r < 4; ++r)
+        #pragma unroll
+        for (int d = 0; d < 4; ++d)
+          sRed[w][((lhi*2 + m)*4 + r)*4 + d] = part[m][r][d];
+  }
+  __syncthreads();
+
+  if (tid < 128) {
     int q = tid >> 2, d = tid & 3;
+    int m = q >> 4, lh = (q >> 2) & 3, r = q & 3;
+    int idx = ((lh*2 + m)*4 + r)*4 + d;
     float a = db2[d];
-    for (int j = 0; j < 256; ++j) a += sH2[q*264 + j] * sDW2[j*4 + d];
+    #pragma unroll
+    for (int ww = 0; ww < 8; ++ww) a += sRed[ww][idx];
     out[(size_t)(q0 + q)*4 + d] = a;
   }
 }
@@ -803,16 +994,15 @@
   ushort* lwL = (ushort*)alloc((size_t)NLAY*1048576*2);
   const size_t qkvO = 0, apO = 196608, gateO = 262144, foO = 786432;
 
+  ushort* featcH = (ushort*)alloc(524288*2);   ushort* featcL = (ushort*)alloc(524288*2);
   ushort* xpH = (ushort*)alloc(1048576*2);
   ushort* xpL = (ushort*)alloc(1048576*2);
   float*  tok = (float*)alloc(262144*4);
   ushort* hH  = (ushort*)alloc(262144*2);
   ushort* hL  = (ushort*)alloc(262144*2);
-  float*  qkvb = (float*)alloc(786432*4);
   ushort* oH  = (ushort*)alloc(262144*2);
   ushort* oL  = (ushort*)alloc(262144*2);
   float*  unionBuf = (float*)alloc(2097152*4);
-  float*  gfeat  = unionBuf;
   float*  projCL = unionBuf + 1048576;
 
   ushort* QsH = (ushort*)unionBuf;
@@ -822,10 +1012,9 @@
   ushort* VtH = QsH + 4*262144;
   ushort* VtL = QsH + 5*262144;
 
-  ushort* featcH = xpH;  ushort* featcL = xpL;
-  ushort* ffH    = xpH;  ushort* ffL    = xpL;
-  ushort* prH    = xpH;  ushort* prL    = xpL;
-  ushort* tkH    = hH;   ushort* tkL    = hL;
+  ushort* ffH = xpH;  ushort* ffL = xpL;
+  ushort* prH = xpH;  ushort* prL = xpL;
+  ushort* tkH = hH;   ushort* tkL = hL;
 
   k_gemm<<<dim3(8,8), 256, 0, stream>>>(pw2, dw1 + 256*256, Wcomb, 256, 256, 512);
   k_beff<<<1, 256, 0, stream>>>(db1, pb2, dw1, b2eff);
@@ -863,27 +1052,27 @@
 
   k_encode<<<dim3(GRD, 2), 256, 0, stream>>>(bpx, bpy, bpi, cellstart, grd,
                                              enc_w1, enc_b1, enc_w2, enc_b2, featcH, featcL);
-  k_mgemm64<true,false><<<dim3(4,64), 256, 0, stream>>>(featcH, featcL, inprojTH, inprojTL, inproj_b, nullptr, gfeat, GRD, 256, 128);
-  k_patchgather<<<4096, 256, 0, stream>>>(gfeat, xpH, xpL);
-  k_mgemm64<true,false><<<dim3(4,16), 256, 0, stream>>>(xpH, xpL, patchTH, patchTL, patch_b, nullptr, tok, TOK, 256, 1024);
+  k_inproj<<<dim3(4,64), 256, 0, stream>>>(featcH, featcL, inprojTH, inprojTL, inproj_b, xpH, xpL);
+  k_mgemm64<true,false,false><<<dim3(4,16), 256, 0, stream>>>(xpH, xpL, patchTH, patchTL, patch_b, nullptr, tok, TOK, 256, 1024, nullptr, nullptr);
 
   for (int l = 0; l < NLAY; ++l) {
     size_t lb = (size_t)l*1048576;
     k_rmsnorm_split<<<TOK, 256, 0, stream>>>(tok, norm1_w + (size_t)l*DIMD, hH, hL);
-    k_mgemm64<false,false><<<dim3(12,16), 256, 0, stream>>>(hH, hL, lwH + lb + qkvO, lwL + lb + qkvO, nullptr, nullptr, qkvb, TOK, 768, 256);
-    k_qkvprep<<<1024, 256, 0, stream>>>(qkvb, QsH, QsL, KsH, KsL, VtH, VtL);
+    k_qkvrope<<<dim3(12,16), 256, 0, stream>>>(hH, hL, lwH + lb + qkvO, lwL + lb + qkvO,
+                                               QsH, QsL, KsH, KsL, VtH, VtL);
     k_fattn<<<256, 512, 0, stream>>>(QsH, QsL, KsH, KsL, VtH, VtL, oH, oL);
-    k_mgemm64<false,true><<<dim3(4,16), 256, 0, stream>>>(oH, oL, lwH + lb + apO, lwL + lb + apO, nullptr, tok, tok, TOK, 256, 256);
+    k_mgemm64<false,true,false><<<dim3(4,16), 256, 0, stream>>>(oH, oL, lwH + lb + apO, lwL + lb + apO, nullptr, tok, tok, TOK, 256, 256, nullptr, nullptr);
     k_rmsnorm_split<<<TOK, 256, 0, stream>>>(tok, norm2_w + (size_t)l*DIMD, hH, hL);
     k_ffgv<<<dim3(16,16), 256, 0, stream>>>(hH, hL, lwH + lb + gateO, lwL + lb + gateO, ffH, ffL);
-    k_mgemm64<false,true><<<dim3(4,16), 256, 0, stream>>>(ffH, ffL, lwH + lb + foO, lwL + lb + foO, nullptr, tok, tok, TOK, 256, 1024);
-  }
-
-  k_split<<<1024, 256, 0, stream>>>(tok, tkH, tkL, 262144);
-  k_mgemm64<true,false><<<dim3(16,16), 256, 0, stream>>>(tkH, tkL, upTH, upTL, unpatch_b, nullptr, gfeat, TOK, 1024, 256);
-  k_unpatch<<<4096, 256, 0, stream>>>(gfeat, prH, prL);
-  k_mgemm64<false,false><<<dim3(4,64), 256, 0, stream>>>(prH, prL, dw1aTH, dw1aTL, nullptr, nullptr, projCL, GRD, 256, 256);
-
-  k_qhead<<<NQ/QN, 256, 0, stream>>>(qpos, quinf, qsdf, qgrad, projCL,
+    if (l < NLAY-1)
+      k_mgemm64<false,true,false><<<dim3(4,16), 256, 0, stream>>>(ffH, ffL, lwH + lb + foO, lwL + lb + foO, nullptr, tok, tok, TOK, 256, 1024, nullptr, nullptr);
+    else
+      k_mgemm64<false,true,true><<<dim3(4,16), 256, 0, stream>>>(ffH, ffL, lwH + lb + foO, lwL + lb + foO, nullptr, tok, tok, TOK, 256, 1024, tkH, tkL);
+  }
+
+  k_upgemm<<<dim3(16,16), 256, 0, stream>>>(tkH, tkL, upTH, upTL, unpatch_b, prH, prL);
+  k_mgemm64<false,false,false><<<dim3(4,64), 256, 0, stream>>>(prH, prL, dw1aTH, dw1aTL, nullptr, nullptr, projCL, GRD, 256, 256, nullptr, nullptr);
+
+  k_qhead<<<NQ/QN, 512, 0, stream>>>(qpos, quinf, qsdf, qgrad, projCL,
       pw1TH, pw1TL, pb1, wcTH, wcTL, b2eff, dw2, db2, out);
 }
```

Measured after the change: 740.1 us. 4.1% less time.
